# Optimization experiments

Measured on AMD Instinct MI355X. Metric: run time of the kernel, lower is better.

Reference implementation:

```python
import jax, jax.numpy as jnp
from jax import lax
import numpy as np

B, N, S, K = 8, 4096, 1024, 32
D_FEAT = 64
EPS = 1e-5


def fps_idx(pts, npoint):
    # pts: [N,3] -> farthest point sampling indices [npoint] (deterministic start at 0)
    n = pts.shape[0]
    def body(i, state):
        dist, far, idxs = state
        idxs = idxs.at[i].set(far)
        d = jnp.sum((pts - pts[far]) ** 2, axis=-1)
        dist = jnp.minimum(dist, d)
        return dist, jnp.argmax(dist).astype(jnp.int32), idxs
    init = (jnp.full((n,), 1e10, pts.dtype), jnp.int32(0), jnp.zeros((npoint,), jnp.int32))
    _, _, idxs = lax.fori_loop(0, npoint, body, init)
    return idxs


def bn(x, g, b, axes, c_axis):
    # batch-norm, training mode (batch statistics), matching torch default module state
    m = jnp.mean(x, axes, keepdims=True)
    v = jnp.var(x, axes, keepdims=True)
    shape = [1] * x.ndim
    shape[c_axis] = -1
    return g.reshape(shape) * (x - m) * lax.rsqrt(v + EPS) + b.reshape(shape)


def conv1x1(x, w, b):
    # x: [B,C,S,K], w: [O,C], b: [O]
    return jnp.einsum('oc,bcsk->bosk', w, x) + b[None, :, None, None]


def setup_inputs():
    key = jax.random.key(0)
    ks = jax.random.split(key, 20)
    p = lambda k, shape: jax.random.normal(k, shape, jnp.float32) * 0.05
    inp = {
        'xyz': jax.random.normal(ks[0], (B, 3, N), jnp.float32),
        'features': jax.random.normal(ks[1], (B, D_FEAT, N), jnp.float32),
        # main MLP: 67 -> 64 -> 64 -> 128
        'w0': p(ks[2], (64, 67)), 'b0': p(ks[3], (64,)), 'g0': jnp.ones(64), 'be0': jnp.zeros(64),
        'w1': p(ks[4], (64, 64)), 'b1': p(ks[5], (64,)), 'g1': jnp.ones(64), 'be1': jnp.zeros(64),
        'w2': p(ks[6], (128, 64)), 'b2': p(ks[7], (128,)), 'g2': jnp.ones(128), 'be2': jnp.zeros(128),
        # WeightNet: 3 -> 8 -> 8 -> 16
        'ww0': p(ks[8], (8, 3)), 'wb0': p(ks[9], (8,)), 'wg0': jnp.ones(8), 'wbe0': jnp.zeros(8),
        'ww1': p(ks[10], (8, 8)), 'wb1': p(ks[11], (8,)), 'wg1': jnp.ones(8), 'wbe1': jnp.zeros(8),
        'ww2': p(ks[12], (16, 8)), 'wb2': p(ks[13], (16,)), 'wg2': jnp.ones(16), 'wbe2': jnp.zeros(16),
        # final linear 16*128 -> 128 and BN1d
        'lw': p(ks[14], (128, 16 * 128)), 'lb': p(ks[15], (128,)),
        'lg': jnp.ones(128), 'lbe': jnp.zeros(128),
    }
    return inp


def reference(xyz, features, w0, b0, g0, be0, w1, b1, g1, be1, w2, b2, g2, be2,
              ww0, wb0, wg0, wbe0, ww1, wb1, wg1, wbe1, ww2, wb2, wg2, wbe2,
              lw, lb, lg, lbe):
    xyz_t = jnp.transpose(xyz, (0, 2, 1))          # [B,N,3]
    feat_t = jnp.transpose(features, (0, 2, 1))    # [B,N,D]

    # farthest point sampling (indices non-differentiable, as in CUDA FPS)
    fidx = jax.vmap(lambda pts: fps_idx(pts, S))(lax.stop_gradient(xyz_t))  # [B,S]
    fps_xyz = jnp.take_along_axis(xyz_t, fidx[..., None], axis=1)           # [B,S,3]

    # KNN: squared distances [B,S,N], take K smallest
    d2 = (jnp.sum(fps_xyz ** 2, -1, keepdims=True)
          + jnp.sum(xyz_t ** 2, -1)[:, None, :]
          - 2.0 * jnp.einsum('bsc,bnc->bsn', fps_xyz, xyz_t))
    _, idx = lax.top_k(-lax.stop_gradient(d2), K)                            # [B,S,K]

    gather = jax.vmap(lambda src, i: src[i])
    grouped_xyz = gather(xyz_t, idx) - fps_xyz[:, :, None, :]                # [B,S,K,3]
    grouped_feat = gather(feat_t, idx)                                       # [B,S,K,D]
    nf = jnp.concatenate([grouped_xyz, grouped_feat], axis=-1)               # [B,S,K,3+D]

    nf = jnp.transpose(nf, (0, 3, 1, 2))                                     # [B,C,S,K]
    for w, b, g, be in ((w0, b0, g0, be0), (w1, b1, g1, be1), (w2, b2, g2, be2)):
        nf = jax.nn.relu(bn(conv1x1(nf, w, b), g, be, (0, 2, 3), 1))

    gx = jnp.transpose(grouped_xyz, (0, 3, 1, 2))                            # [B,3,S,K]
    wts = gx
    for w, b, g, be in ((ww0, wb0, wg0, wbe0), (ww1, wb1, wg1, wbe1), (ww2, wb2, wg2, wbe2)):
        wts = jax.nn.relu(bn(conv1x1(wts, w, b), g, be, (0, 2, 3), 1))       # [B,16,S,K]

    agg = jnp.einsum('bdsk,bcsk->bsdc', nf, wts)                             # [B,S,128,16]
    agg = agg.reshape(agg.shape[0], agg.shape[1], -1)                        # [B,S,2048] (D outer, C inner)
    lin = agg @ lw.T + lb                                                    # [B,S,128]
    lin = jnp.transpose(lin, (0, 2, 1))                                      # [B,128,S]
    out_f = jax.nn.relu(bn(lin, lg, lbe, (0, 2), 1))

    new_xyz = jnp.transpose(fps_xyz, (0, 2, 1))                              # [B,3,S]
    return (new_xyz, out_f)
```

## Files before the change

kernel.cpp:

```cpp
#include <hip/hip_runtime.h>
#include <hip/hip_bf16.h>

#define BB 8
#define NN 4096
#define SS 1024
#define KK 32
#define PP (BB*SS*KK)

typedef unsigned long long u64;
typedef unsigned int u32;
typedef unsigned short u16;
typedef float f32x2 __attribute__((ext_vector_type(2)));

#define ST_Y0 0
#define ST_W0 64
#define ST_Y1 72
#define ST_W1 136
#define ST_Y2 144
#define ST_W2 272
#define ST_LIN 288

static __device__ __forceinline__ float bf2f(u32 u){ return __uint_as_float(u<<16); }
static __device__ __forceinline__ u16 f2bf(float f){ u32 u=__float_as_uint(f); return (u16)((u + 0x7FFFu + ((u>>16)&1u))>>16); }

static __device__ __forceinline__ f32x2 pk_add(f32x2 a, f32x2 b){
  f32x2 d; asm("v_pk_add_f32 %0, %1, %2" : "=v"(d) : "v"(a), "v"(b)); return d;
}
static __device__ __forceinline__ f32x2 pk_mul(f32x2 a, f32x2 b){
  f32x2 d; asm("v_pk_mul_f32 %0, %1, %2" : "=v"(d) : "v"(a), "v"(b)); return d;
}

static __device__ __forceinline__ uint4 pack8(const float* v){
  uint4 r;
  r.x=(u32)f2bf(v[0])|((u32)f2bf(v[1])<<16);
  r.y=(u32)f2bf(v[2])|((u32)f2bf(v[3])<<16);
  r.z=(u32)f2bf(v[4])|((u32)f2bf(v[5])<<16);
  r.w=(u32)f2bf(v[6])|((u32)f2bf(v[7])<<16);
  return r;
}

static __device__ __forceinline__ void unp8_aff(uint4 r, const float* A, const float* C, int cb, float* o){
  o[0]=fmaxf(fmaf(bf2f(r.x&0xffffu),A[cb+0],C[cb+0]),0.f);
  o[1]=fmaxf(fmaf(bf2f(r.x>>16)    ,A[cb+1],C[cb+1]),0.f);
  o[2]=fmaxf(fmaf(bf2f(r.y&0xffffu),A[cb+2],C[cb+2]),0.f);
  o[3]=fmaxf(fmaf(bf2f(r.y>>16)    ,A[cb+3],C[cb+3]),0.f);
  o[4]=fmaxf(fmaf(bf2f(r.z&0xffffu),A[cb+4],C[cb+4]),0.f);
  o[5]=fmaxf(fmaf(bf2f(r.z>>16)    ,A[cb+5],C[cb+5]),0.f);
  o[6]=fmaxf(fmaf(bf2f(r.w&0xffffu),A[cb+6],C[cb+6]),0.f);
  o[7]=fmaxf(fmaf(bf2f(r.w>>16)    ,A[cb+7],C[cb+7]),0.f);
}

template<int CTRL, int RMASK>
static __device__ __forceinline__ u32 dppmax(u32 m){
  u32 t=(u32)__builtin_amdgcn_update_dpp(0, (int)m, CTRL, RMASK, 0xf, false);
  return t>m ? t : m;
}
template<int CTRL, int RMASK>
static __device__ __forceinline__ float dppadd1(float v){
  float t=__uint_as_float((u32)__builtin_amdgcn_update_dpp(0,(int)__float_as_uint(v),CTRL,RMASK,0xf,false));
  return v+t;
}
static __device__ __forceinline__ float dppsum(float v){
  v=dppadd1<0x111,0xf>(v);
  v=dppadd1<0x112,0xf>(v);
  v=dppadd1<0x114,0xf>(v);
  v=dppadd1<0x118,0xf>(v);
  v=dppadd1<0x142,0xa>(v);
  v=dppadd1<0x143,0xc>(v);
  return v;
}
static __device__ __forceinline__ float rl63(float v){
  return __uint_as_float((u32)__builtin_amdgcn_readlane((int)__float_as_uint(v),63));
}

__global__ __launch_bounds__(512) void k_fps_ft(const float* __restrict__ xyz,
    float* __restrict__ fpsq, float* __restrict__ outx,
    const float* __restrict__ f, float* __restrict__ ft,
    const float* __restrict__ w0,const float* __restrict__ w1,const float* __restrict__ w2,
    const float* __restrict__ ww0,const float* __restrict__ ww1,const float* __restrict__ ww2,
    float* __restrict__ w0t,float* __restrict__ w1t,float* __restrict__ w2t,
    float* __restrict__ wt0,float* __restrict__ wt1,float* __restrict__ wt2,
    float* __restrict__ statsf){
  __shared__ union USm {
    struct { float X[NN],Y[NN],Z[NN]; float QX[SS],QY[SS],QZ[SS]; u64 red[2][8]; } a;
    float tile[2][64][65];
  } sm;
  int blk=blockIdx.x; int t=threadIdx.x;
  if (blk>=8){
    if (blk==264){
      for (int i=t;i<1024;i+=512) statsf[i]=0.f;
      for (int i=t;i<64*67;i+=512){ int o=i/67,k=i%67; w0t[k*64+o]=w0[i]; }
      for (int i=t;i<64*64;i+=512){ int o=i>>6,k=i&63; w1t[k*64+o]=w1[i]; }
      for (int i=t;i<128*64;i+=512){ int o=i>>6,k=i&63; w2t[k*128+o]=w2[i]; }
      for (int i=t;i<8*3;i+=512){ int o=i/3,k=i%3; wt0[k*8+o]=ww0[i]; }
      for (int i=t;i<8*8;i+=512){ int o=i>>3,k=i&7; wt1[k*8+o]=ww1[i]; }
      for (int i=t;i<16*8;i+=512){ int o=i>>3,k=i&7; wt2[k*16+o]=ww2[i]; }
      return;
    }
    int sub=t>>8, tt=t&255;
    int tileIdx=(blk-8)*2+sub;
    int b=tileIdx>>6; int n0=(tileIdx&63)*64;
    const float* fb=f+(size_t)b*64*NN;
    int c0=tt>>6, nn=tt&63;
    #pragma unroll
    for (int it=0;it<16;it++){ int c=c0+it*4; sm.tile[sub][c][nn]=fb[(size_t)c*NN+n0+nn]; }
    __syncthreads();
    int cc=tt&63, n1=tt>>6;
    float* fo=ft+((size_t)b*NN+n0)*64;
    #pragma unroll
    for (int it=0;it<16;it++){ int n=n1+it*4; fo[(size_t)n*64+cc]=sm.tile[sub][cc][n]; }
    return;
  }
  float* X=sm.a.X; float* Y=sm.a.Y; float* Z=sm.a.Z;
  float* QX=sm.a.QX; float* QY=sm.a.QY; float* QZ=sm.a.QZ;
  int b=blk;
  const float* xb=xyz+(size_t)b*3*NN;
  for (int i=t;i<NN;i+=512){ X[i]=xb[i]; Y[i]=xb[NN+i]; Z[i]=xb[2*NN+i]; }
  __syncthreads();
  f32x2 px[4],py[4],pz[4],dd[4];
  #pragma unroll
  for (int k=0;k<4;k++){
    int i=t*8+2*k;
    px[k].x=X[i]; px[k].y=X[i+1];
    py[k].x=Y[i]; py[k].y=Y[i+1];
    pz[k].x=Z[i]; pz[k].y=Z[i+1];
    dd[k].x=1e10f; dd[k].y=1e10f;
  }
  int wv=t>>6, ln=t&63;
  int far=0;
  for (int s=0;s<SS;s++){
    float fx=X[far], fy=Y[far], fz=Z[far];
    if (t==0){ QX[s]=fx; QY[s]=fy; QZ[s]=fz; }
    f32x2 nfx, nfy, nfz;
    nfx.x=-fx; nfx.y=-fx; nfy.x=-fy; nfy.y=-fy; nfz.x=-fz; nfz.y=-fz;
    #pragma unroll
    for (int k=0;k<4;k++){
      f32x2 dx=pk_add(px[k],nfx);
      f32x2 xx=pk_mul(dx,dx);
      f32x2 dy=pk_add(py[k],nfy);
      f32x2 yy=pk_mul(dy,dy);
      f32x2 dz=pk_add(pz[k],nfz);
      f32x2 zz=pk_mul(dz,dz);
      f32x2 s1=pk_add(xx,yy);
      f32x2 d2=pk_add(s1,zz);
      dd[k].x=fminf(dd[k].x,d2.x);
      dd[k].y=fminf(dd[k].y,d2.y);
    }
    float m01=fmaxf(dd[0].x,dd[0].y), m23=fmaxf(dd[1].x,dd[1].y);
    float m45=fmaxf(dd[2].x,dd[2].y), m67=fmaxf(dd[3].x,dd[3].y);
    u32 m=__float_as_uint(fmaxf(fmaxf(m01,m23),fmaxf(m45,m67)));
    m=dppmax<0x111,0xf>(m);
    m=dppmax<0x112,0xf>(m);
    m=dppmax<0x114,0xf>(m);
    m=dppmax<0x118,0xf>(m);
    u32 r15=(u32)__builtin_amdgcn_readlane((int)m,15);
    u32 r31=(u32)__builtin_amdgcn_readlane((int)m,31);
    u32 r47=(u32)__builtin_amdgcn_readlane((int)m,47);
    u32 r63=(u32)__builtin_amdgcn_readlane((int)m,63);
    u32 ab = r15>r31 ? r15 : r31;
    u32 cd = r47>r63 ? r47 : r63;
    u32 wmax = ab>cd ? ab : cd;
    int lj=8;
    if (__float_as_uint(dd[3].y)==wmax) lj=7;
    if (__float_as_uint(dd[3].x)==wmax) lj=6;
    if (__float_as_uint(dd[2].y)==wmax) lj=5;
    if (__float_as_uint(dd[2].x)==wmax) lj=4;
    if (__float_as_uint(dd[1].y)==wmax) lj=3;
    if (__float_as_uint(dd[1].x)==wmax) lj=2;
    if (__float_as_uint(dd[0].y)==wmax) lj=1;
    if (__float_as_uint(dd[0].x)==wmax) lj=0;
    u64 ball=__ballot(lj<8);
    u32 wl=(u32)__builtin_ctzll(ball);
    int gi=t*8+lj;
    u32 widx=(u32)__builtin_amdgcn_readlane(gi,wl);
    int pb=s&1;
    if (ln==0) sm.a.red[pb][wv]=((u64)wmax<<32)|(u32)(4095u-widx);
    __syncthreads();
    const double* rd=(const double*)&sm.a.red[pb][0];
    double g=fmax(fmax(fmax(rd[0],rd[1]),fmax(rd[2],rd[3])),
                  fmax(fmax(rd[4],rd[5]),fmax(rd[6],rd[7])));
    far=4095-(int)(__double_as_longlong(g)&0xFFFull);
  }
  __syncthreads();
  for (int i=t;i<SS;i+=512){
    float qx=QX[i], qy=QY[i], qz=QZ[i];
    float* q=&fpsq[((size_t)b*SS+i)*3]; q[0]=qx; q[1]=qy; q[2]=qz;
    outx[b*3*SS+i]=qx; outx[b*3*SS+SS+i]=qy; outx[b*3*SS+2*SS+i]=qz;
  }
}

#define KSTR 68
__global__ __launch_bounds__(256) void k_knn(const float* __restrict__ xyz, const float* __restrict__ fpsq,
                                             int* __restrict__ kidx){
  extern __shared__ char smem[];
  float* xs=(float*)smem;
  float* ys=xs+64*KSTR;
  float* zs=ys+64*KSTR;
  float* pn=zs+64*KSTR;
  int blk=blockIdx.x; int b=blk>>8; int s0=(blk&255)*4;
  const float* xb=xyz+(size_t)b*3*NN;
  for (int i=threadIdx.x;i<NN;i+=256){
    float x=xb[i],y=xb[NN+i],z=xb[2*NN+i];
    int slot=(i>>6)*KSTR+(i&63);
    xs[slot]=x; ys[slot]=y; zs[slot]=z;
    pn[slot]=__fadd_rn(__fadd_rn(__fmul_rn(x,x),__fmul_rn(y,y)),__fmul_rn(z,z));
  }
  __syncthreads();
  int wv=threadIdx.x>>6, ln=threadIdx.x&63;
  int s=s0+wv;
  const float* q=&fpsq[((size_t)b*SS+s)*3];
  float qx=q[0],qy=q[1],qz=q[2];
  float qn=__fadd_rn(__fadd_rn(__fmul_rn(qx,qx),__fmul_rn(qy,qy)),__fmul_rn(qz,qz));
  f32x2 qxx,qyy,qzz,qnn,mtwo;
  qxx.x=qx;qxx.y=qx; qyy.x=qy;qyy.y=qy; qzz.x=qz;qzz.y=qz; qnn.x=qn;qnn.y=qn;
  mtwo.x=-2.f; mtwo.y=-2.f;
  const float4* Xp=(const float4*)(xs+ln*KSTR);
  const float4* Yp=(const float4*)(ys+ln*KSTR);
  const float4* Zp=(const float4*)(zs+ln*KSTR);
  const float4* Pp=(const float4*)(pn+ln*KSTR);
  int base=ln*64;
  u64 v[64];
  #pragma unroll
  for (int g=0;g<16;g++){
    float4 x4=Xp[g], y4=Yp[g], z4=Zp[g], p4=Pp[g];
    #pragma unroll
    for (int h=0;h<2;h++){
      f32x2 px2,py2,pz2,pn2;
      if (h==0){ px2.x=x4.x;px2.y=x4.y; py2.x=y4.x;py2.y=y4.y; pz2.x=z4.x;pz2.y=z4.y; pn2.x=p4.x;pn2.y=p4.y; }
      else     { px2.x=x4.z;px2.y=x4.w; py2.x=y4.z;py2.y=y4.w; pz2.x=z4.z;pz2.y=z4.w; pn2.x=p4.z;pn2.y=p4.w; }
      f32x2 m1=pk_mul(qxx,px2);
      f32x2 mm=pk_mul(qyy,py2);
      f32x2 a1=pk_add(m1,mm);
      f32x2 m3=pk_mul(qzz,pz2);
      f32x2 dt=pk_add(a1,m3);
      f32x2 qp=pk_add(qnn,pn2);
      f32x2 nd=pk_mul(dt,mtwo);
      f32x2 d2=pk_add(qp,nd);
      #pragma unroll
      for (int e=0;e<2;e++){
        u32 bu=__float_as_uint(e?d2.y:d2.x);
        bu = ((int)bu<0)? ~bu : (bu|0x80000000u);
        v[g*4+h*2+e]=((u64)bu<<32)|(u32)(base+g*4+h*2+e);
      }
    }
  }
  u64 cand[8];
  #pragma unroll
  for (int gg=0;gg<8;gg++){
    u64 c=v[gg*8];
    #pragma unroll
    for (int j=1;j<8;j++){ u64 x=v[gg*8+j]; c = x<c?x:c; }
    cand[gg]=c;
  }
  u64 best=cand[0];
  #pragma unroll
  for (int gg=1;gg<8;gg++){ u64 x=cand[gg]; best = x<best?x:best; }
  int my=0;
  #pragma unroll 1
  for (int r=0;r<KK;r++){
    u64 w=best;
    #pragma unroll
    for (int m=1;m<64;m<<=1){ u64 o=__shfl_xor(w,m,64); w = o<w?o:w; }
    if (ln==r) my=(int)(w&0xFFFull);
    if (best==w){
      #pragma unroll
      for (int gg=0;gg<8;gg++){
        if (cand[gg]==w){
          u64 c=~0ull;
          #pragma unroll
          for (int j=0;j<8;j++){ u64 x=v[gg*8+j]; x = x>w ? x : ~0ull; c = x<c?x:c; }
          cand[gg]=c;
        }
      }
      u64 nb=cand[0];
      #pragma unroll
      for (int gg=1;gg<8;gg++){ u64 x=cand[gg]; nb = x<nb?x:nb; }
      best=nb;
    }
  }
  if (ln<KK) kidx[(((size_t)b*SS+s)<<5)+ln]=my;
}

__global__ __launch_bounds__(256) void k_l0(const float* __restrict__ xyz, const float* __restrict__ ft,
    const float* __restrict__ fpsq, const int* __restrict__ kidx,
    const float* __restrict__ w0t, const float* __restrict__ wt0,
    u16* __restrict__ y0, float* __restrict__ wl0, float* __restrict__ statsf){
  __shared__ u16 ytile[256][64];
  __shared__ float pS[4][64], pQ[4][64];
  __shared__ float pWS[4][8], pWQ[4][8];
  int t=threadIdx.x; int wv=t>>6, ln=t&63;
  int p=blockIdx.x*256+t;
  int b=p>>15;
  int site=p>>5;
  int j=kidx[p];
  const float* xb=xyz+(size_t)b*3*NN;
  const float* q=fpsq+(size_t)site*3;
  float gx=xb[j]-q[0], gy=xb[NN+j]-q[1], gz=xb[2*NN+j]-q[2];
  float acc[64];
  #pragma unroll
  for (int c=0;c<64;c++) acc[c]=fmaf(gx,w0t[c],fmaf(gy,w0t[64+c],gz*w0t[128+c]));
  const float4* fr=(const float4*)(ft+((size_t)b*NN+j)*64);
  #pragma unroll 1
  for (int kb=0;kb<4;kb++){
    float4 r0=fr[kb*4+0], r1=fr[kb*4+1], r2=fr[kb*4+2], r3=fr[kb*4+3];
    float ch[16]={r0.x,r0.y,r0.z,r0.w,r1.x,r1.y,r1.z,r1.w,r2.x,r2.y,r2.z,r2.w,r3.x,r3.y,r3.z,r3.w};
    const float* wb=w0t+(3+kb*16)*64;
    #pragma unroll
    for (int kk=0;kk<16;kk++){
      #pragma unroll
      for (int c=0;c<64;c++) acc[c]=fmaf(ch[kk],wb[kk*64+c],acc[c]);
    }
  }
  u16* yr=y0+(size_t)p*64;
  #pragma unroll
  for (int c8=0;c8<8;c8++){
    uint4 pk=pack8(&acc[c8*8]);
    ((uint4*)yr)[c8]=pk;
    *((uint4*)&ytile[t][c8*8])=pk;
  }
  float wa[8];
  #pragma unroll
  for (int o=0;o<8;o++) wa[o]=fmaf(gx,wt0[o],fmaf(gy,wt0[8+o],gz*wt0[16+o]));
  float4* wr=(float4*)(wl0+(size_t)p*8);
  wr[0]=make_float4(wa[0],wa[1],wa[2],wa[3]);
  wr[1]=make_float4(wa[4],wa[5],wa[6],wa[7]);
  float wS[8],wQ[8];
  #pragma unroll
  for (int o=0;o<8;o++){
    wS[o]=rl63(dppsum(wa[o]));
    wQ[o]=rl63(dppsum(wa[o]*wa[o]));
  }
  if (ln==0){
    #pragma unroll
    for (int o=0;o<8;o++){ pWS[wv][o]=wS[o]; pWQ[wv][o]=wQ[o]; }
  }
  __syncthreads();
  {
    int c=t&63, rg=t>>6;
    float S=0.f,Q=0.f;
    #pragma unroll 16
    for (int r=0;r<64;r++){
      float v=bf2f((u32)ytile[rg*64+r][c]);
      S+=v; Q=fmaf(v,v,Q);
    }
    pS[rg][c]=S; pQ[rg][c]=Q;
  }
  __syncthreads();
  if (t<64){
    float S=pS[0][t]+pS[1][t]+pS[2][t]+pS[3][t];
    float Q=pQ[0][t]+pQ[1][t]+pQ[2][t]+pQ[3][t];
    atomicAdd(&statsf[2*(ST_Y0+t)],S); atomicAdd(&statsf[2*(ST_Y0+t)+1],Q);
  } else if (t<72){
    int c=t-64;
    float S=pWS[0][c]+pWS[1][c]+pWS[2][c]+pWS[3][c];
    float Q=pWQ[0][c]+pWQ[1][c]+pWQ[2][c]+pWQ[3][c];
    atomicAdd(&statsf[2*(ST_W0+c)],S); atomicAdd(&statsf[2*(ST_W0+c)+1],Q);
  }
}

__global__ __launch_bounds__(256) void k_l1(const u16* __restrict__ y0, const float* __restrict__ wl0,
    const float* __restrict__ w1t, const float* __restrict__ wt1,
    const float* __restrict__ statsf,
    const float* __restrict__ g0v, const float* __restrict__ be0v,
    const float* __restrict__ wg0v, const float* __restrict__ wbe0v,
    u16* __restrict__ y1, float* __restrict__ wl1, float* __restrict__ statso){
  __shared__ float A0[64],C0[64],AW[8],CW[8];
  __shared__ u16 ytile[256][64];
  __shared__ float pS[4][64], pQ[4][64];
  __shared__ float pWS[4][8], pWQ[4][8];
  int t=threadIdx.x; int wv=t>>6, ln=t&63;
  if (t<64){
    float sm=statsf[(ST_Y0+t)*2], sq=statsf[(ST_Y0+t)*2+1];
    float mean=sm*(1.f/PP), var=fmaxf(sq*(1.f/PP)-mean*mean,0.f);
    float a=g0v[t]*rsqrtf(var+1e-5f); A0[t]=a; C0[t]=be0v[t]-mean*a;
  } else if (t<72){
    int c=t-64;
    float sm=statsf[(ST_W0+c)*2], sq=statsf[(ST_W0+c)*2+1];
    float mean=sm*(1.f/PP), var=fmaxf(sq*(1.f/PP)-mean*mean,0.f);
    float a=wg0v[c]*rsqrtf(var+1e-5f); AW[c]=a; CW[c]=wbe0v[c]-mean*a;
  }
  __syncthreads();
  int p=blockIdx.x*256+t;
  const uint4* yr=(const uint4*)(y0+(size_t)p*64);
  float acc[64];
  #pragma unroll
  for (int c=0;c<64;c++) acc[c]=0.f;
  #pragma unroll 1
  for (int kb=0;kb<4;kb++){
    uint4 r0=yr[kb*2], r1=yr[kb*2+1];
    float ch[16];
    unp8_aff(r0,A0,C0,kb*16,ch);
    unp8_aff(r1,A0,C0,kb*16+8,ch+8);
    const float* wb=w1t+kb*16*64;
    #pragma unroll
    for (int kk=0;kk<16;kk++){
      #pragma unroll
      for (int c=0;c<64;c++) acc[c]=fmaf(ch[kk],wb[kk*64+c],acc[c]);
    }
  }
  u16* yo=y1+(size_t)p*64;
  #pragma unroll
  for (int c8=0;c8<8;c8++){
    uint4 pk=pack8(&acc[c8*8]);
    ((uint4*)yo)[c8]=pk;
    *((uint4*)&ytile[t][c8*8])=pk;
  }
  const float4* wvp=(const float4*)(wl0+(size_t)p*8);
  float4 v0=wvp[0], v1=wvp[1];
  float wi[8]={v0.x,v0.y,v0.z,v0.w,v1.x,v1.y,v1.z,v1.w};
  float wo[8];
  #pragma unroll
  for (int o=0;o<8;o++) wo[o]=0.f;
  #pragma unroll
  for (int k=0;k<8;k++){
    float xr=fmaxf(fmaf(wi[k],AW[k],CW[k]),0.f);
    #pragma unroll
    for (int o=0;o<8;o++) wo[o]=fmaf(xr,wt1[k*8+o],wo[o]);
  }
  float4* wr=(float4*)(wl1+(size_t)p*8);
  wr[0]=make_float4(wo[0],wo[1],wo[2],wo[3]);
  wr[1]=make_float4(wo[4],wo[5],wo[6],wo[7]);
  float wS[8],wQ[8];
  #pragma unroll
  for (int o=0;o<8;o++){
    wS[o]=rl63(dppsum(wo[o]));
    wQ[o]=rl63(dppsum(wo[o]*wo[o]));
  }
  if (ln==0){
    #pragma unroll
    for (int o=0;o<8;o++){ pWS[wv][o]=wS[o]; pWQ[wv][o]=wQ[o]; }
  }
  __syncthreads();
  {
    int c=t&63, rg=t>>6;
    float S=0.f,Q=0.f;
    #pragma unroll 16
    for (int r=0;r<64;r++){
      float v=bf2f((u32)ytile[rg*64+r][c]);
      S+=v; Q=fmaf(v,v,Q);
    }
    pS[rg][c]=S; pQ[rg][c]=Q;
  }
  __syncthreads();
  if (t<64){
    float S=pS[0][t]+pS[1][t]+pS[2][t]+pS[3][t];
    float Q=pQ[0][t]+pQ[1][t]+pQ[2][t]+pQ[3][t];
    atomicAdd(&statso[2*(ST_Y1+t)],S); atomicAdd(&statso[2*(ST_Y1+t)+1],Q);
  } else if (t<72){
    int c=t-64;
    float S=pWS[0][c]+pWS[1][c]+pWS[2][c]+pWS[3][c];
    float Q=pWQ[0][c]+pWQ[1][c]+pWQ[2][c]+pWQ[3][c];
    atomicAdd(&statso[2*(ST_W1+c)],S); atomicAdd(&statso[2*(ST_W1+c)+1],Q);
  }
}

__global__ __launch_bounds__(256) void k_l2(const u16* __restrict__ y1, const float* __restrict__ wl1,
    const float* __restrict__ w2t, const float* __restrict__ wt2,
    const float* __restrict__ statsf,
    const float* __restrict__ g1v, const float* __restrict__ be1v,
    const float* __restrict__ wg1v, const float* __restrict__ wbe1v,
    u16* __restrict__ y2, float* __restrict__ wl2, float* __restrict__ statso){
  __shared__ float A1[64],C1[64],AW[8],CW[8];
  __shared__ u16 ytile[256][64];
  __shared__ float pS[4][64], pQ[4][64];
  __shared__ float pWS[4][16], pWQ[4][16];
  int t=threadIdx.x; int wv=t>>6, ln=t&63;
  if (t<64){
    float sm=statsf[(ST_Y1+t)*2], sq=statsf[(ST_Y1+t)*2+1];
    float mean=sm*(1.f/PP), var=fmaxf(sq*(1.f/PP)-mean*mean,0.f);
    float a=g1v[t]*rsqrtf(var+1e-5f); A1[t]=a; C1[t]=be1v[t]-mean*a;
  } else if (t<72){
    int c=t-64;
    float sm=statsf[(ST_W1+c)*2], sq=statsf[(ST_W1+c)*2+1];
    float mean=sm*(1.f/PP), var=fmaxf(sq*(1.f/PP)-mean*mean,0.f);
    float a=wg1v[c]*rsqrtf(var+1e-5f); AW[c]=a; CW[c]=wbe1v[c]-mean*a;
  }
  __syncthreads();
  int p=blockIdx.x*256+t;
  const uint4* yr=(const uint4*)(y1+(size_t)p*64);
  #pragma unroll 1
  for (int h=0;h<2;h++){
    float acc[64];
    #pragma unroll
    for (int c=0;c<64;c++) acc[c]=0.f;
    #pragma unroll 1
    for (int kb=0;kb<4;kb++){
      uint4 r0=yr[kb*2], r1=yr[kb*2+1];
      float ch[16];
      unp8_aff(r0,A1,C1,kb*16,ch);
      unp8_aff(r1,A1,C1,kb*16+8,ch+8);
      const float* wb=w2t+(size_t)kb*16*128+h*64;
      #pragma unroll
      for (int kk=0;kk<16;kk++){
        #pragma unroll
        for (int c=0;c<64;c++) acc[c]=fmaf(ch[kk],wb[kk*128+c],acc[c]);
      }
    }
    u16* yo=y2+(size_t)p*128+h*64;
    #pragma unroll
    for (int c8=0;c8<8;c8++){
      uint4 pk=pack8(&acc[c8*8]);
      ((uint4*)yo)[c8]=pk;
      *((uint4*)&ytile[t][c8*8])=pk;
    }
    __syncthreads();
    {
      int c=t&63, rg=t>>6;
      float S=0.f,Q=0.f;
      #pragma unroll 16
      for (int r=0;r<64;r++){
        float v=bf2f((u32)ytile[rg*64+r][c]);
        S+=v; Q=fmaf(v,v,Q);
      }
      pS[rg][c]=S; pQ[rg][c]=Q;
    }
    __syncthreads();
    if (t<64){
      float S=pS[0][t]+pS[1][t]+pS[2][t]+pS[3][t];
      float Q=pQ[0][t]+pQ[1][t]+pQ[2][t]+pQ[3][t];
      atomicAdd(&statso[2*(ST_Y2+h*64+t)],S); atomicAdd(&statso[2*(ST_Y2+h*64+t)+1],Q);
    }
    __syncthreads();
  }
  const float4* wvp=(const float4*)(wl1+(size_t)p*8);
  float4 v0=wvp[0], v1=wvp[1];
  float wi[8]={v0.x,v0.y,v0.z,v0.w,v1.x,v1.y,v1.z,v1.w};
  float wo[16];
  #pragma unroll
  for (int o=0;o<16;o++) wo[o]=0.f;
  #pragma unroll
  for (int k=0;k<8;k++){
    float xr=fmaxf(fmaf(wi[k],AW[k],CW[k]),0.f);
    #pragma unroll
    for (int o=0;o<16;o++) wo[o]=fmaf(xr,wt2[k*16+o],wo[o]);
  }
  float4* wr=(float4*)(wl2+(size_t)p*16);
  wr[0]=make_float4(wo[0],wo[1],wo[2],wo[3]);
  wr[1]=make_float4(wo[4],wo[5],wo[6],wo[7]);
  wr[2]=make_float4(wo[8],wo[9],wo[10],wo[11]);
  wr[3]=make_float4(wo[12],wo[13],wo[14],wo[15]);
  float wS[16],wQ[16];
  #pragma unroll
  for (int o=0;o<16;o++){
    wS[o]=rl63(dppsum(wo[o]));
    wQ[o]=rl63(dppsum(wo[o]*wo[o]));
  }
  if (ln==0){
    #pragma unroll
    for (int o=0;o<16;o++){ pWS[wv][o]=wS[o]; pWQ[wv][o]=wQ[o]; }
  }
  __syncthreads();
  if (t<16){
    float S=pWS[0][t]+pWS[1][t]+pWS[2][t]+pWS[3][t];
    float Q=pWQ[0][t]+pWQ[1][t]+pWQ[2][t]+pWQ[3][t];
    atomicAdd(&statso[2*(ST_W2+t)],S); atomicAdd(&statso[2*(ST_W2+t)+1],Q);
  }
}

__global__ __launch_bounds__(256) void k_agg(const u16* __restrict__ y2, const float* __restrict__ wl2,
    const float* __restrict__ statsf,
    const float* __restrict__ g2v, const float* __restrict__ be2v,
    const float* __restrict__ wg2v, const float* __restrict__ wbe2v,
    u16* __restrict__ agg){
  __shared__ float A2[128],C2[128],AW[16],CW[16];
  __shared__ float nf[32*128];
  __shared__ float wt[32*16];
  int site=blockIdx.x; int t=threadIdx.x;
  if (t<128){
    float sm=statsf[(ST_Y2+t)*2], sq=statsf[(ST_Y2+t)*2+1];
    float mean=sm*(1.f/PP), var=fmaxf(sq*(1.f/PP)-mean*mean,0.f);
    float a=g2v[t]*rsqrtf(var+1e-5f); A2[t]=a; C2[t]=be2v[t]-mean*a;
  } else if (t<144){
    int c=t-128;
    float sm=statsf[(ST_W2+c)*2], sq=statsf[(ST_W2+c)*2+1];
    float mean=sm*(1.f/PP), var=fmaxf(sq*(1.f/PP)-mean*mean,0.f);
    float a=wg2v[c]*rsqrtf(var+1e-5f); AW[c]=a; CW[c]=wbe2v[c]-mean*a;
  }
  __syncthreads();
  const uint4* src=(const uint4*)(y2+(size_t)site*32*128);
  #pragma unroll
  for (int it=0;it<2;it++){
    int idx=t+it*256;
    uint4 r=src[idx];
    int base=(idx*8)&127; int kq=(idx*8)>>7;
    unp8_aff(r,A2,C2,base,&nf[kq*128+base]);
  }
  #pragma unroll
  for (int it=0;it<2;it++){
    int i=t+it*256;
    float x=wl2[(size_t)site*512+i]; int c=i&15;
    wt[i]=fmaxf(fmaf(x,AW[c],CW[c]),0.f);
  }
  __syncthreads();
  int d=t>>1, cb=(t&1)*8;
  float acc[8];
  #pragma unroll
  for (int e=0;e<8;e++) acc[e]=0.f;
  #pragma unroll 4
  for (int kq=0;kq<32;kq++){
    float nv=nf[kq*128+d];
    #pragma unroll
    for (int e=0;e<8;e++) acc[e]=fmaf(nv,wt[kq*16+cb+e],acc[e]);
  }
  ((uint4*)(agg+(size_t)site*2048))[t]=pack8(acc);
}

__global__ __launch_bounds__(256) void k_lin(const u16* __restrict__ agg, const float* __restrict__ lw,
                                             float* __restrict__ lin, float* __restrict__ outst){
  __shared__ float As[32][33];
  __shared__ float Bs[32][128];
  __shared__ float stS[8][132], stQ[8][132];
  int s0=blockIdx.x*32; int t=threadIdx.x;
  int tx=t&31, ty=t>>5;
  float acc[4][4];
  #pragma unroll
  for (int i=0;i<4;i++){
    #pragma unroll
    for (int jj=0;jj<4;jj++) acc[i][jj]=0.f;
  }
  for (int kb=0;kb<2048;kb+=32){
    {
      int row=t>>3, kc=(t&7)*4;
      uint2 raw=*(const uint2*)(agg+((size_t)(s0+row))*2048+kb+kc);
      As[row][kc  ]=bf2f(raw.x&0xffffu); As[row][kc+1]=bf2f(raw.x>>16);
      As[row][kc+2]=bf2f(raw.y&0xffffu); As[row][kc+3]=bf2f(raw.y>>16);
    }
    {
      int o=t>>1, ks=(t&1)*16;
      const float* lr=lw+(size_t)o*2048+kb+ks;
      #pragma unroll
      for (int i=0;i<16;i+=4){
        float4 r=*(const float4*)(lr+i);
        Bs[ks+i][o]=r.x; Bs[ks+i+1][o]=r.y; Bs[ks+i+2][o]=r.z; Bs[ks+i+3][o]=r.w;
      }
    }
    __syncthreads();
    #pragma unroll 8
    for (int kk=0;kk<32;kk++){
      float av[4];
      #pragma unroll
      for (int i=0;i<4;i++) av[i]=As[ty*4+i][kk];
      float4 bv=*(const float4*)(&Bs[kk][tx*4]);
      #pragma unroll
      for (int i=0;i<4;i++){
        acc[i][0]=fmaf(av[i],bv.x,acc[i][0]);
        acc[i][1]=fmaf(av[i],bv.y,acc[i][1]);
        acc[i][2]=fmaf(av[i],bv.z,acc[i][2]);
        acc[i][3]=fmaf(av[i],bv.w,acc[i][3]);
      }
    }
    __syncthreads();
  }
  #pragma unroll
  for (int i=0;i<4;i++){
    float4 o4=make_float4(acc[i][0],acc[i][1],acc[i][2],acc[i][3]);
    *(float4*)(lin+((size_t)(s0+ty*4+i))*128+tx*4)=o4;
  }
  #pragma unroll
  for (int jj=0;jj<4;jj++){
    float a0=acc[0][jj],a1=acc[1][jj],a2=acc[2][jj],a3=acc[3][jj];
    stS[ty][tx*4+jj]=(a0+a1)+(a2+a3);
    stQ[ty][tx*4+jj]=fmaf(a3,a3,fmaf(a2,a2,fmaf(a1,a1,a0*a0)));
  }
  __syncthreads();
  if (t<128){
    float S=0.f,Q=0.f;
    #pragma unroll
    for (int k=0;k<8;k++){ S+=stS[k][t]; Q+=stQ[k][t]; }
    atomicAdd(&outst[2*t],S); atomicAdd(&outst[2*t+1],Q);
  }
}

__global__ __launch_bounds__(256) void k_out(const float* __restrict__ lin, const float* __restrict__ statsf,
    const float* __restrict__ lg, const float* __restrict__ lbe, float* __restrict__ outf){
  int t=blockIdx.x*256+threadIdx.x;
  int s4=(t&255)*4; int o=(t>>8)&127; int b=t>>15;
  float sm=statsf[(ST_LIN+o)*2], sq=statsf[(ST_LIN+o)*2+1];
  float mean=sm*(1.f/8192.f), var=fmaxf(sq*(1.f/8192.f)-mean*mean,0.f);
  float a=lg[o]*rsqrtf(var+1e-5f), cc=lbe[o]-mean*a;
  float v0=lin[((size_t)b*SS+s4+0)*128+o];
  float v1=lin[((size_t)b*SS+s4+1)*128+o];
  float v2=lin[((size_t)b*SS+s4+2)*128+o];
  float v3=lin[((size_t)b*SS+s4+3)*128+o];
  float4 r=make_float4(fmaxf(fmaf(v0,a,cc),0.f),fmaxf(fmaf(v1,a,cc),0.f),
                       fmaxf(fmaf(v2,a,cc),0.f),fmaxf(fmaf(v3,a,cc),0.f));
  *(float4*)(outf+((size_t)b*128+o)*SS+s4)=r;
}

extern "C" void kernel_launch(void* const* d_in, const int* in_sizes, int n_in,
                              void* d_out, int out_size, void* d_ws, size_t ws_size,
                              hipStream_t stream){
  (void)in_sizes;(void)n_in;(void)out_size;(void)ws_size;
  const float* xyz =(const float*)d_in[0];
  const float* feat=(const float*)d_in[1];
  const float* w0=(const float*)d_in[2];  const float* g0=(const float*)d_in[4];  const float* be0=(const float*)d_in[5];
  const float* w1=(const float*)d_in[6];  const float* g1=(const float*)d_in[8];  const float* be1=(const float*)d_in[9];
  const float* w2=(const float*)d_in[10]; const float* g2=(const float*)d_in[12]; const float* be2=(const float*)d_in[13];
  const float* ww0=(const float*)d_in[14]; const float* wg0=(const float*)d_in[16]; const float* wbe0=(const float*)d_in[17];
  const float* ww1=(const float*)d_in[18]; const float* wg1=(const float*)d_in[20]; const float* wbe1=(const float*)d_in[21];
  const float* ww2=(const float*)d_in[22]; const float* wg2=(const float*)d_in[24]; const float* wbe2=(const float*)d_in[25];
  const float* lw=(const float*)d_in[26]; const float* lg=(const float*)d_in[28]; const float* lbe=(const float*)d_in[29];
  float* out=(float*)d_out;
  char* ws=(char*)d_ws;

  size_t cur=0;
  auto alloc=[&](size_t bytes)->size_t{ cur=(cur+255)&~(size_t)255; size_t o=cur; cur+=bytes; return o; };
  size_t o_stats=alloc(4096);
  size_t o_w0t =alloc(67*64*4);
  size_t o_w1t =alloc(64*64*4);
  size_t o_w2t =alloc(64*128*4);
  size_t o_wt0 =alloc(3*8*4);
  size_t o_wt1 =alloc(8*8*4);
  size_t o_wt2 =alloc(8*16*4);
  size_t o_fpsq=alloc((size_t)BB*SS*3*4);
  size_t o_kidx=alloc((size_t)PP*4);
  size_t o_ft  =alloc((size_t)BB*NN*64*4);
  size_t o_y0  =alloc((size_t)PP*64*2);
  size_t o_y1  =alloc((size_t)PP*64*2);
  size_t o_y2  =alloc((size_t)PP*128*2);
  size_t o_wl0 =alloc((size_t)PP*8*4);
  size_t o_wl1 =alloc((size_t)PP*8*4);
  size_t o_wl2 =alloc((size_t)PP*16*4);
  size_t o_agg =alloc((size_t)8192*2048*2);
  size_t o_lin =alloc((size_t)8192*128*4);

  float* statsf=(float*)(ws+o_stats);
  float* w0t=(float*)(ws+o_w0t); float* w1t=(float*)(ws+o_w1t); float* w2t=(float*)(ws+o_w2t);
  float* wt0=(float*)(ws+o_wt0); float* wt1=(float*)(ws+o_wt1); float* wt2=(float*)(ws+o_wt2);
  float* fpsq=(float*)(ws+o_fpsq); int* kidx=(int*)(ws+o_kidx);
  float* ft=(float*)(ws+o_ft);
  u16* y0=(u16*)(ws+o_y0); u16* y1=(u16*)(ws+o_y1); u16* y2=(u16*)(ws+o_y2);
  float* wl0=(float*)(ws+o_wl0); float* wl1=(float*)(ws+o_wl1); float* wl2=(float*)(ws+o_wl2);
  u16* agg=(u16*)(ws+o_agg); float* lin=(float*)(ws+o_lin);

  size_t knn_smem = (size_t)4*64*KSTR*4;

  hipLaunchKernelGGL(k_fps_ft,dim3(265),dim3(512),0,stream,xyz,fpsq,out,feat,ft,
                     w0,w1,w2,ww0,ww1,ww2,w0t,w1t,w2t,wt0,wt1,wt2,statsf);
  hipLaunchKernelGGL(k_knn,dim3(2048),dim3(256),knn_smem,stream,xyz,fpsq,kidx);
  hipLaunchKernelGGL(k_l0,dim3(PP/256),dim3(256),0,stream,xyz,ft,fpsq,kidx,w0t,wt0,y0,wl0,statsf);
  hipLaunchKernelGGL(k_l1,dim3(PP/256),dim3(256),0,stream,y0,wl0,w1t,wt1,statsf,g0,be0,wg0,wbe0,y1,wl1,statsf);
  hipLaunchKernelGGL(k_l2,dim3(PP/256),dim3(256),0,stream,y1,wl1,w2t,wt2,statsf,g1,be1,wg1,wbe1,y2,wl2,statsf);
  hipLaunchKernelGGL(k_agg,dim3(8192),dim3(256),0,stream,y2,wl2,statsf,g2,be2,wg2,wbe2,agg);
  hipLaunchKernelGGL(k_lin,dim3(256),dim3(256),0,stream,agg,lw,lin,statsf+2*ST_LIN);
  hipLaunchKernelGGL(k_out,dim3(1024),dim3(256),0,stream,lin,statsf,lg,lbe,out+BB*3*SS);
}
```

Measured before the change: 1.315 ms.

## Fuse all stages into one cooperative persistent kernel with grid syncs

Replaces the eight separate kernel launches with a single cooperative kernel of 256 blocks of 512 threads that runs FPS, kNN, the three MLP layers, aggregation, the linear layer and the output BN in sequence, separated by grid.sync. The aim is to remove launch gaps and per-kernel tail effects. Work is remapped onto the fixed grid, with two passes per stage and kNN handling 32 queries per block. The cost is that 248 blocks sit idle during the long serial FPS phase, and the smaller grid may lower occupancy and parallelism in the heavier stages.

After: 2.262 ms. 71.9% more time.

```diff
diff --git a/kernel.cpp b/kernel.cpp
--- a/kernel.cpp
+++ b/kernel.cpp
@@ -1,5 +1,8 @@
 #include <hip/hip_runtime.h>
 #include <hip/hip_bf16.h>
+#include <hip/hip_cooperative_groups.h>
+
+namespace cg = cooperative_groups;
 
 #define BB 8
 #define NN 4096
@@ -20,8 +23,13 @@
 #define ST_W2 272
 #define ST_LIN 288
 
+#define DLDS 69632
+#define KSTR 68
+
 static __device__ __forceinline__ float bf2f(u32 u){ return __uint_as_float(u<<16); }
 static __device__ __forceinline__ u16 f2bf(float f){ u32 u=__float_as_uint(f); return (u16)((u + 0x7FFFu + ((u>>16)&1u))>>16); }
+
+static __device__ __forceinline__ float aread(float* p){ return atomicAdd(p, 0.0f); }
 
 static __device__ __forceinline__ f32x2 pk_add(f32x2 a, f32x2 b){
   f32x2 d; asm("v_pk_add_f32 %0, %1, %2" : "=v"(d) : "v"(a), "v"(b)); return d;
@@ -73,21 +81,129 @@
   return __uint_as_float((u32)__builtin_amdgcn_readlane((int)__float_as_uint(v),63));
 }
 
-__global__ __launch_bounds__(512) void k_fps_ft(const float* __restrict__ xyz,
-    float* __restrict__ fpsq, float* __restrict__ outx,
-    const float* __restrict__ f, float* __restrict__ ft,
+__global__ __launch_bounds__(512,2) void k_mega(
+    const float* __restrict__ xyz, const float* __restrict__ feat,
     const float* __restrict__ w0,const float* __restrict__ w1,const float* __restrict__ w2,
     const float* __restrict__ ww0,const float* __restrict__ ww1,const float* __restrict__ ww2,
-    float* __restrict__ w0t,float* __restrict__ w1t,float* __restrict__ w2t,
-    float* __restrict__ wt0,float* __restrict__ wt1,float* __restrict__ wt2,
-    float* __restrict__ statsf){
-  __shared__ union USm {
-    struct { float X[NN],Y[NN],Z[NN]; float QX[SS],QY[SS],QZ[SS]; u64 red[2][8]; } a;
-    float tile[2][64][65];
-  } sm;
-  int blk=blockIdx.x; int t=threadIdx.x;
-  if (blk>=8){
-    if (blk==264){
+    const float* __restrict__ g0,const float* __restrict__ be0,
+    const float* __restrict__ g1,const float* __restrict__ be1,
+    const float* __restrict__ g2,const float* __restrict__ be2,
+    const float* __restrict__ wg0,const float* __restrict__ wbe0,
+    const float* __restrict__ wg1,const float* __restrict__ wbe1,
+    const float* __restrict__ wg2,const float* __restrict__ wbe2,
+    const float* __restrict__ lw,const float* __restrict__ lg,const float* __restrict__ lbe,
+    float* out,
+    float* fpsq, int* kidx, float* ft,
+    u16* y0, u16* y1, u16* y2,
+    float* wl0, float* wl1, float* wl2,
+    u16* aggb, float* lin, float* statsf,
+    float* w0t, float* w1t, float* w2t,
+    float* wt0, float* wt1, float* wt2){
+  extern __shared__ char dsm[];
+  __shared__ union SSM {
+    u64 red[2][8];
+    struct { float pS[8][64], pQ[8][64], pWS[8][16], pWQ[8][16];
+             float A[64], C[64], AW[8], CW[8]; } st;
+    struct { float A[128], C[128], AW[16], CW[16]; } bn;
+    struct { float S[128], Q2[128]; } ln;
+  } ssm;
+  cg::grid_group grid = cg::this_grid();
+  const int blk=blockIdx.x, t=threadIdx.x;
+  const int wv=t>>6, ln=t&63;
+
+  if (blk<8){
+    float* X=(float*)dsm; float* Y=X+NN; float* Z=Y+NN;
+    float* QX=Z+NN; float* QY=QX+SS; float* QZ=QY+SS;
+    const float* xb=xyz+(size_t)blk*3*NN;
+    for (int i=t;i<NN;i+=512){ X[i]=xb[i]; Y[i]=xb[NN+i]; Z[i]=xb[2*NN+i]; }
+    __syncthreads();
+    f32x2 px[4],py[4],pz[4],dd[4];
+    #pragma unroll
+    for (int k=0;k<4;k++){
+      int i=t*8+2*k;
+      px[k].x=X[i]; px[k].y=X[i+1];
+      py[k].x=Y[i]; py[k].y=Y[i+1];
+      pz[k].x=Z[i]; pz[k].y=Z[i+1];
+      dd[k].x=1e10f; dd[k].y=1e10f;
+    }
+    int far=0;
+    for (int s=0;s<SS;s++){
+      float fx=X[far], fy=Y[far], fz=Z[far];
+      if (t==0){ QX[s]=fx; QY[s]=fy; QZ[s]=fz; }
+      f32x2 nfx, nfy, nfz;
+      nfx.x=-fx; nfx.y=-fx; nfy.x=-fy; nfy.y=-fy; nfz.x=-fz; nfz.y=-fz;
+      #pragma unroll
+      for (int k=0;k<4;k++){
+        f32x2 dx=pk_add(px[k],nfx);
+        f32x2 xx=pk_mul(dx,dx);
+        f32x2 dy=pk_add(py[k],nfy);
+        f32x2 yy=pk_mul(dy,dy);
+        f32x2 dz=pk_add(pz[k],nfz);
+        f32x2 zz=pk_mul(dz,dz);
+        f32x2 s1=pk_add(xx,yy);
+        f32x2 d2=pk_add(s1,zz);
+        dd[k].x=fminf(dd[k].x,d2.x);
+        dd[k].y=fminf(dd[k].y,d2.y);
+      }
+      float m01=fmaxf(dd[0].x,dd[0].y), m23=fmaxf(dd[1].x,dd[1].y);
+      float m45=fmaxf(dd[2].x,dd[2].y), m67=fmaxf(dd[3].x,dd[3].y);
+      u32 m=__float_as_uint(fmaxf(fmaxf(m01,m23),fmaxf(m45,m67)));
+      m=dppmax<0x111,0xf>(m);
+      m=dppmax<0x112,0xf>(m);
+      m=dppmax<0x114,0xf>(m);
+      m=dppmax<0x118,0xf>(m);
+      u32 r15=(u32)__builtin_amdgcn_readlane((int)m,15);
+      u32 r31=(u32)__builtin_amdgcn_readlane((int)m,31);
+      u32 r47=(u32)__builtin_amdgcn_readlane((int)m,47);
+      u32 r63=(u32)__builtin_amdgcn_readlane((int)m,63);
+      u32 ab = r15>r31 ? r15 : r31;
+      u32 cd = r47>r63 ? r47 : r63;
+      u32 wmax = ab>cd ? ab : cd;
+      int lj=8;
+      if (__float_as_uint(dd[3].y)==wmax) lj=7;
+      if (__float_as_uint(dd[3].x)==wmax) lj=6;
+      if (__float_as_uint(dd[2].y)==wmax) lj=5;
+      if (__float_as_uint(dd[2].x)==wmax) lj=4;
+      if (__float_as_uint(dd[1].y)==wmax) lj=3;
+      if (__float_as_uint(dd[1].x)==wmax) lj=2;
+      if (__float_as_uint(dd[0].y)==wmax) lj=1;
+      if (__float_as_uint(dd[0].x)==wmax) lj=0;
+      u64 ball=__ballot(lj<8);
+      u32 wl=(u32)__builtin_ctzll(ball);
+      int gi=t*8+lj;
+      u32 widx=(u32)__builtin_amdgcn_readlane(gi,wl);
+      int pb=s&1;
+      if (ln==0) ssm.red[pb][wv]=((u64)wmax<<32)|(u32)(4095u-widx);
+      __syncthreads();
+      const double* rd=(const double*)&ssm.red[pb][0];
+      double g=fmax(fmax(fmax(rd[0],rd[1]),fmax(rd[2],rd[3])),
+                    fmax(fmax(rd[4],rd[5]),fmax(rd[6],rd[7])));
+      far=4095-(int)(__double_as_longlong(g)&0xFFFull);
+    }
+    __syncthreads();
+    for (int i=t;i<SS;i+=512){
+      float qx=QX[i], qy=QY[i], qz=QZ[i];
+      float* q=&fpsq[((size_t)blk*SS+i)*3]; q[0]=qx; q[1]=qy; q[2]=qz;
+      out[blk*3*SS+i]=qx; out[blk*3*SS+SS+i]=qy; out[blk*3*SS+2*SS+i]=qz;
+    }
+  } else {
+    float (*tile)[64][65]=(float(*)[64][65])dsm;
+    int sub=t>>8, tt=t&255;
+    for (int base=blk-8; base<256; base+=248){
+      int tileIdx=base*2+sub;
+      int b=tileIdx>>6; int n0=(tileIdx&63)*64;
+      const float* fb=feat+(size_t)b*64*NN;
+      int c0=tt>>6, nn=tt&63;
+      #pragma unroll
+      for (int it=0;it<16;it++){ int c=c0+it*4; tile[sub][c][nn]=fb[(size_t)c*NN+n0+nn]; }
+      __syncthreads();
+      int cc=tt&63, n1=tt>>6;
+      float* fo=ft+((size_t)b*NN+n0)*64;
+      #pragma unroll
+      for (int it=0;it<16;it++){ int n=n1+it*4; fo[(size_t)n*64+cc]=tile[sub][cc][n]; }
+      __syncthreads();
+    }
+    if (blk==254){
       for (int i=t;i<1024;i+=512) statsf[i]=0.f;
       for (int i=t;i<64*67;i+=512){ int o=i/67,k=i%67; w0t[k*64+o]=w0[i]; }
       for (int i=t;i<64*64;i+=512){ int o=i>>6,k=i&63; w1t[k*64+o]=w1[i]; }
@@ -95,596 +211,497 @@
       for (int i=t;i<8*3;i+=512){ int o=i/3,k=i%3; wt0[k*8+o]=ww0[i]; }
       for (int i=t;i<8*8;i+=512){ int o=i>>3,k=i&7; wt1[k*8+o]=ww1[i]; }
       for (int i=t;i<16*8;i+=512){ int o=i>>3,k=i&7; wt2[k*16+o]=ww2[i]; }
-      return;
-    }
+    }
+  }
+  __threadfence(); grid.sync();
+
+  {
+    float* xs=(float*)dsm;
+    float* ys=xs+64*KSTR;
+    float* zs=ys+64*KSTR;
+    float* pn=zs+64*KSTR;
+    int b=blk>>5; int q0=(blk&31)<<5;
+    const float* xb=xyz+(size_t)b*3*NN;
+    for (int i=t;i<NN;i+=512){
+      float x=xb[i],y=xb[NN+i],z=xb[2*NN+i];
+      int slot=(i>>6)*KSTR+(i&63);
+      xs[slot]=x; ys[slot]=y; zs[slot]=z;
+      pn[slot]=__fadd_rn(__fadd_rn(__fmul_rn(x,x),__fmul_rn(y,y)),__fmul_rn(z,z));
+    }
+    __syncthreads();
+    const float4* Xp=(const float4*)(xs+ln*KSTR);
+    const float4* Yp=(const float4*)(ys+ln*KSTR);
+    const float4* Zp=(const float4*)(zs+ln*KSTR);
+    const float4* Pp=(const float4*)(pn+ln*KSTR);
+    int base=ln*64;
+    #pragma unroll 1
+    for (int pass=0;pass<4;pass++){
+      int s=q0+pass*8+wv;
+      const float* q=&fpsq[((size_t)b*SS+s)*3];
+      float qx=q[0],qy=q[1],qz=q[2];
+      float qn=__fadd_rn(__fadd_rn(__fmul_rn(qx,qx),__fmul_rn(qy,qy)),__fmul_rn(qz,qz));
+      f32x2 qxx,qyy,qzz,qnn,mtwo;
+      qxx.x=qx;qxx.y=qx; qyy.x=qy;qyy.y=qy; qzz.x=qz;qzz.y=qz; qnn.x=qn;qnn.y=qn;
+      mtwo.x=-2.f; mtwo.y=-2.f;
+      u64 v[64];
+      #pragma unroll
+      for (int g=0;g<16;g++){
+        float4 x4=Xp[g], y4=Yp[g], z4=Zp[g], p4=Pp[g];
+        #pragma unroll
+        for (int h=0;h<2;h++){
+          f32x2 px2,py2,pz2,pn2;
+          if (h==0){ px2.x=x4.x;px2.y=x4.y; py2.x=y4.x;py2.y=y4.y; pz2.x=z4.x;pz2.y=z4.y; pn2.x=p4.x;pn2.y=p4.y; }
+          else     { px2.x=x4.z;px2.y=x4.w; py2.x=y4.z;py2.y=y4.w; pz2.x=z4.z;pz2.y=z4.w; pn2.x=p4.z;pn2.y=p4.w; }
+          f32x2 m1=pk_mul(qxx,px2);
+          f32x2 mm=pk_mul(qyy,py2);
+          f32x2 a1=pk_add(m1,mm);
+          f32x2 m3=pk_mul(qzz,pz2);
+          f32x2 dt=pk_add(a1,m3);
+          f32x2 qp=pk_add(qnn,pn2);
+          f32x2 nd=pk_mul(dt,mtwo);
+          f32x2 d2=pk_add(qp,nd);
+          #pragma unroll
+          for (int e=0;e<2;e++){
+            u32 bu=__float_as_uint(e?d2.y:d2.x);
+            bu = ((int)bu<0)? ~bu : (bu|0x80000000u);
+            v[g*4+h*2+e]=((u64)bu<<32)|(u32)(base+g*4+h*2+e);
+          }
+        }
+      }
+      u64 cand[8];
+      #pragma unroll
+      for (int gg=0;gg<8;gg++){
+        u64 c=v[gg*8];
+        #pragma unroll
+        for (int j=1;j<8;j++){ u64 x=v[gg*8+j]; c = x<c?x:c; }
+        cand[gg]=c;
+      }
+      u64 best=cand[0];
+      #pragma unroll
+      for (int gg=1;gg<8;gg++){ u64 x=cand[gg]; best = x<best?x:best; }
+      int my=0;
+      #pragma unroll 1
+      for (int r=0;r<KK;r++){
+        u64 w=best;
+        #pragma unroll
+        for (int m=1;m<64;m<<=1){ u64 o=__shfl_xor(w,m,64); w = o<w?o:w; }
+        if (ln==r) my=(int)(w&0xFFFull);
+        if (best==w){
+          #pragma unroll
+          for (int gg=0;gg<8;gg++){
+            if (cand[gg]==w){
+              u64 c=~0ull;
+              #pragma unroll
+              for (int j=0;j<8;j++){ u64 x=v[gg*8+j]; x = x>w ? x : ~0ull; c = x<c?x:c; }
+              cand[gg]=c;
+            }
+          }
+          u64 nb=cand[0];
+          #pragma unroll
+          for (int gg=1;gg<8;gg++){ u64 x=cand[gg]; nb = x<nb?x:nb; }
+          best=nb;
+        }
+      }
+      if (ln<KK) kidx[(((size_t)b*SS+s)<<5)+ln]=my;
+    }
+  }
+  __threadfence(); grid.sync();
+
+  {
+    u16 (*ytile)[64]=(u16(*)[64])dsm;
+    #pragma unroll 1
+    for (int pass=0;pass<2;pass++){
+      int p=blk*512+t+pass*131072;
+      int b=p>>15;
+      int site=p>>5;
+      int j=kidx[p];
+      const float* xb=xyz+(size_t)b*3*NN;
+      const float* q=fpsq+(size_t)site*3;
+      float gx=xb[j]-q[0], gy=xb[NN+j]-q[1], gz=xb[2*NN+j]-q[2];
+      float acc[64];
+      #pragma unroll
+      for (int c=0;c<64;c++) acc[c]=fmaf(gx,w0t[c],fmaf(gy,w0t[64+c],gz*w0t[128+c]));
+      const float4* fr=(const float4*)(ft+((size_t)b*NN+j)*64);
+      #pragma unroll 1
+      for (int kb=0;kb<4;kb++){
+        float4 r0=fr[kb*4+0], r1=fr[kb*4+1], r2=fr[kb*4+2], r3=fr[kb*4+3];
+        float ch[16]={r0.x,r0.y,r0.z,r0.w,r1.x,r1.y,r1.z,r1.w,r2.x,r2.y,r2.z,r2.w,r3.x,r3.y,r3.z,r3.w};
+        const float* wb=w0t+(3+kb*16)*64;
+        #pragma unroll
+        for (int kk=0;kk<16;kk++){
+          #pragma unroll
+          for (int c=0;c<64;c++) acc[c]=fmaf(ch[kk],wb[kk*64+c],acc[c]);
+        }
+      }
+      u16* yr=y0+(size_t)p*64;
+      #pragma unroll
+      for (int c8=0;c8<8;c8++){
+        uint4 pk=pack8(&acc[c8*8]);
+        ((uint4*)yr)[c8]=pk;
+        *((uint4*)&ytile[t][c8*8])=pk;
+      }
+      float wa[8];
+      #pragma unroll
+      for (int o=0;o<8;o++) wa[o]=fmaf(gx,wt0[o],fmaf(gy,wt0[8+o],gz*wt0[16+o]));
+      float4* wr=(float4*)(wl0+(size_t)p*8);
+      wr[0]=make_float4(wa[0],wa[1],wa[2],wa[3]);
+      wr[1]=make_float4(wa[4],wa[5],wa[6],wa[7]);
+      float wS[8],wQ[8];
+      #pragma unroll
+      for (int o=0;o<8;o++){
+        wS[o]=rl63(dppsum(wa[o]));
+        wQ[o]=rl63(dppsum(wa[o]*wa[o]));
+      }
+      if (ln==0){
+        #pragma unroll
+        for (int o=0;o<8;o++){ ssm.st.pWS[wv][o]=wS[o]; ssm.st.pWQ[wv][o]=wQ[o]; }
+      }
+      __syncthreads();
+      {
+        int c=t&63, rg=t>>6;
+        float S=0.f,Q=0.f;
+        #pragma unroll 16
+        for (int r=0;r<64;r++){
+          float v=bf2f((u32)ytile[rg*64+r][c]);
+          S+=v; Q=fmaf(v,v,Q);
+        }
+        ssm.st.pS[rg][c]=S; ssm.st.pQ[rg][c]=Q;
+      }
+      __syncthreads();
+      if (t<64){
+        float S=0.f,Q=0.f;
+        #pragma unroll
+        for (int w=0;w<8;w++){ S+=ssm.st.pS[w][t]; Q+=ssm.st.pQ[w][t]; }
+        atomicAdd(&statsf[2*(ST_Y0+t)],S); atomicAdd(&statsf[2*(ST_Y0+t)+1],Q);
+      } else if (t<72){
+        int c=t-64;
+        float S=0.f,Q=0.f;
+        #pragma unroll
+        for (int w=0;w<8;w++){ S+=ssm.st.pWS[w][c]; Q+=ssm.st.pWQ[w][c]; }
+        atomicAdd(&statsf[2*(ST_W0+c)],S); atomicAdd(&statsf[2*(ST_W0+c)+1],Q);
+      }
+      __syncthreads();
+    }
+  }
+  __threadfence(); grid.sync();
+
+  {
+    u16 (*ytile)[64]=(u16(*)[64])dsm;
+    if (t<64){
+      float sm=aread(&statsf[(ST_Y0+t)*2]), sq=aread(&statsf[(ST_Y0+t)*2+1]);
+      float mean=sm*(1.f/PP), var=fmaxf(sq*(1.f/PP)-mean*mean,0.f);
+      float a=g0[t]*rsqrtf(var+1e-5f); ssm.st.A[t]=a; ssm.st.C[t]=be0[t]-mean*a;
+    } else if (t<72){
+      int c=t-64;
+      float sm=aread(&statsf[(ST_W0+c)*2]), sq=aread(&statsf[(ST_W0+c)*2+1]);
+      float mean=sm*(1.f/PP), var=fmaxf(sq*(1.f/PP)-mean*mean,0.f);
+      float a=wg0[c]*rsqrtf(var+1e-5f); ssm.st.AW[c]=a; ssm.st.CW[c]=wbe0[c]-mean*a;
+    }
+    __syncthreads();
+    #pragma unroll 1
+    for (int pass=0;pass<2;pass++){
+      int p=blk*512+t+pass*131072;
+      const uint4* yr=(const uint4*)(y0+(size_t)p*64);
+      float acc[64];
+      #pragma unroll
+      for (int c=0;c<64;c++) acc[c]=0.f;
+      #pragma unroll 1
+      for (int kb=0;kb<4;kb++){
+        uint4 r0=yr[kb*2], r1=yr[kb*2+1];
+        float ch[16];
+        unp8_aff(r0,ssm.st.A,ssm.st.C,kb*16,ch);
+        unp8_aff(r1,ssm.st.A,ssm.st.C,kb*16+8,ch+8);
+        const float* wb=w1t+kb*16*64;
+        #pragma unroll
+        for (int kk=0;kk<16;kk++){
+          #pragma unroll
+          for (int c=0;c<64;c++) acc[c]=fmaf(ch[kk],wb[kk*64+c],acc[c]);
+        }
+      }
+      u16* yo=y1+(size_t)p*64;
+      #pragma unroll
+      for (int c8=0;c8<8;c8++){
+        uint4 pk=pack8(&acc[c8*8]);
+        ((uint4*)yo)[c8]=pk;
+        *((uint4*)&ytile[t][c8*8])=pk;
+      }
+      const float4* wvp=(const float4*)(wl0+(size_t)p*8);
+      float4 v0=wvp[0], v1=wvp[1];
+      float wi[8]={v0.x,v0.y,v0.z,v0.w,v1.x,v1.y,v1.z,v1.w};
+      float wo[8];
+      #pragma unroll
+      for (int o=0;o<8;o++) wo[o]=0.f;
+      #pragma unroll
+      for (int k=0;k<8;k++){
+        float xr=fmaxf(fmaf(wi[k],ssm.st.AW[k],ssm.st.CW[k]),0.f);
+        #pragma unroll
+        for (int o=0;o<8;o++) wo[o]=fmaf(xr,wt1[k*8+o],wo[o]);
+      }
+      float4* wr=(float4*)(wl1+(size_t)p*8);
+      wr[0]=make_float4(wo[0],wo[1],wo[2],wo[3]);
+      wr[1]=make_float4(wo[4],wo[5],wo[6],wo[7]);
+      float wS[8],wQ[8];
+      #pragma unroll
+      for (int o=0;o<8;o++){
+        wS[o]=rl63(dppsum(wo[o]));
+        wQ[o]=rl63(dppsum(wo[o]*wo[o]));
+      }
+      if (ln==0){
+        #pragma unroll
+        for (int o=0;o<8;o++){ ssm.st.pWS[wv][o]=wS[o]; ssm.st.pWQ[wv][o]=wQ[o]; }
+      }
+      __syncthreads();
+      {
+        int c=t&63, rg=t>>6;
+        float S=0.f,Q=0.f;
+        #pragma unroll 16
+        for (int r=0;r<64;r++){
+          float v=bf2f((u32)ytile[rg*64+r][c]);
+          S+=v; Q=fmaf(v,v,Q);
+        }
+        ssm.st.pS[rg][c]=S; ssm.st.pQ[rg][c]=Q;
+      }
+      __syncthreads();
+      if (t<64){
+        float S=0.f,Q=0.f;
+        #pragma unroll
+        for (int w=0;w<8;w++){ S+=ssm.st.pS[w][t]; Q+=ssm.st.pQ[w][t]; }
+        atomicAdd(&statsf[2*(ST_Y1+t)],S); atomicAdd(&statsf[2*(ST_Y1+t)+1],Q);
+      } else if (t<72){
+        int c=t-64;
+        float S=0.f,Q=0.f;
+        #pragma unroll
+        for (int w=0;w<8;w++){ S+=ssm.st.pWS[w][c]; Q+=ssm.st.pWQ[w][c]; }
+        atomicAdd(&statsf[2*(ST_W1+c)],S); atomicAdd(&statsf[2*(ST_W1+c)+1],Q);
+      }
+      __syncthreads();
+    }
+  }
+  __threadfence(); grid.sync();
+
+  {
+    u16 (*ytile)[64]=(u16(*)[64])dsm;
+    if (t<64){
+      float sm=aread(&statsf[(ST_Y1+t)*2]), sq=aread(&statsf[(ST_Y1+t)*2+1]);
+      float mean=sm*(1.f/PP), var=fmaxf(sq*(1.f/PP)-mean*mean,0.f);
+      float a=g1[t]*rsqrtf(var+1e-5f); ssm.st.A[t]=a; ssm.st.C[t]=be1[t]-mean*a;
+    } else if (t<72){
+      int c=t-64;
+      float sm=aread(&statsf[(ST_W1+c)*2]), sq=aread(&statsf[(ST_W1+c)*2+1]);
+      float mean=sm*(1.f/PP), var=fmaxf(sq*(1.f/PP)-mean*mean,0.f);
+      float a=wg1[c]*rsqrtf(var+1e-5f); ssm.st.AW[c]=a; ssm.st.CW[c]=wbe1[c]-mean*a;
+    }
+    __syncthreads();
+    #pragma unroll 1
+    for (int pass=0;pass<2;pass++){
+      int p=blk*512+t+pass*131072;
+      const uint4* yr=(const uint4*)(y1+(size_t)p*64);
+      #pragma unroll 1
+      for (int h=0;h<2;h++){
+        float acc[64];
+        #pragma unroll
+        for (int c=0;c<64;c++) acc[c]=0.f;
+        #pragma unroll 1
+        for (int kb=0;kb<4;kb++){
+          uint4 r0=yr[kb*2], r1=yr[kb*2+1];
+          float ch[16];
+          unp8_aff(r0,ssm.st.A,ssm.st.C,kb*16,ch);
+          unp8_aff(r1,ssm.st.A,ssm.st.C,kb*16+8,ch+8);
+          const float* wb=w2t+(size_t)kb*16*128+h*64;
+          #pragma unroll
+          for (int kk=0;kk<16;kk++){
+            #pragma unroll
+            for (int c=0;c<64;c++) acc[c]=fmaf(ch[kk],wb[kk*128+c],acc[c]);
+          }
+        }
+        u16* yo=y2+(size_t)p*128+h*64;
+        #pragma unroll
+        for (int c8=0;c8<8;c8++){
+          uint4 pk=pack8(&acc[c8*8]);
+          ((uint4*)yo)[c8]=pk;
+          *((uint4*)&ytile[t][c8*8])=pk;
+        }
+        __syncthreads();
+        {
+          int c=t&63, rg=t>>6;
+          float S=0.f,Q=0.f;
+          #pragma unroll 16
+          for (int r=0;r<64;r++){
+            float v=bf2f((u32)ytile[rg*64+r][c]);
+            S+=v; Q=fmaf(v,v,Q);
+          }
+          ssm.st.pS[rg][c]=S; ssm.st.pQ[rg][c]=Q;
+        }
+        __syncthreads();
+        if (t<64){
+          float S=0.f,Q=0.f;
+          #pragma unroll
+          for (int w=0;w<8;w++){ S+=ssm.st.pS[w][t]; Q+=ssm.st.pQ[w][t]; }
+          atomicAdd(&statsf[2*(ST_Y2+h*64+t)],S); atomicAdd(&statsf[2*(ST_Y2+h*64+t)+1],Q);
+        }
+        __syncthreads();
+      }
+      const float4* wvp=(const float4*)(wl1+(size_t)p*8);
+      float4 v0=wvp[0], v1=wvp[1];
+      float wi[8]={v0.x,v0.y,v0.z,v0.w,v1.x,v1.y,v1.z,v1.w};
+      float wo[16];
+      #pragma unroll
+      for (int o=0;o<16;o++) wo[o]=0.f;
+      #pragma unroll
+      for (int k=0;k<8;k++){
+        float xr=fmaxf(fmaf(wi[k],ssm.st.AW[k],ssm.st.CW[k]),0.f);
+        #pragma unroll
+        for (int o=0;o<16;o++) wo[o]=fmaf(xr,wt2[k*16+o],wo[o]);
+      }
+      float4* wr=(float4*)(wl2+(size_t)p*16);
+      wr[0]=make_float4(wo[0],wo[1],wo[2],wo[3]);
+      wr[1]=make_float4(wo[4],wo[5],wo[6],wo[7]);
+      wr[2]=make_float4(wo[8],wo[9],wo[10],wo[11]);
+      wr[3]=make_float4(wo[12],wo[13],wo[14],wo[15]);
+      float wS[16],wQ[16];
+      #pragma unroll
+      for (int o=0;o<16;o++){
+        wS[o]=rl63(dppsum(wo[o]));
+        wQ[o]=rl63(dppsum(wo[o]*wo[o]));
+      }
+      if (ln==0){
+        #pragma unroll
+        for (int o=0;o<16;o++){ ssm.st.pWS[wv][o]=wS[o]; ssm.st.pWQ[wv][o]=wQ[o]; }
+      }
+      __syncthreads();
+      if (t<16){
+        float S=0.f,Q=0.f;
+        #pragma unroll
+        for (int w=0;w<8;w++){ S+=ssm.st.pWS[w][t]; Q+=ssm.st.pWQ[w][t]; }
+        atomicAdd(&statsf[2*(ST_W2+t)],S); atomicAdd(&statsf[2*(ST_W2+t)+1],Q);
+      }
+      __syncthreads();
+    }
+  }
+  __threadfence(); grid.sync();
+
+  {
+    if (t<128){
+      float sm=aread(&statsf[(ST_Y2+t)*2]), sq=aread(&statsf[(ST_Y2+t)*2+1]);
+      float mean=sm*(1.f/PP), var=fmaxf(sq*(1.f/PP)-mean*mean,0.f);
+      float a=g2[t]*rsqrtf(var+1e-5f); ssm.bn.A[t]=a; ssm.bn.C[t]=be2[t]-mean*a;
+    } else if (t<144){
+      int c=t-128;
+      float sm=aread(&statsf[(ST_W2+c)*2]), sq=aread(&statsf[(ST_W2+c)*2+1]);
+      float mean=sm*(1.f/PP), var=fmaxf(sq*(1.f/PP)-mean*mean,0.f);
+      float a=wg2[c]*rsqrtf(var+1e-5f); ssm.bn.AW[c]=a; ssm.bn.CW[c]=wbe2[c]-mean*a;
+    }
+    __syncthreads();
     int sub=t>>8, tt=t&255;
-    int tileIdx=(blk-8)*2+sub;
-    int b=tileIdx>>6; int n0=(tileIdx&63)*64;
-    const float* fb=f+(size_t)b*64*NN;
-    int c0=tt>>6, nn=tt&63;
-    #pragma unroll
-    for (int it=0;it<16;it++){ int c=c0+it*4; sm.tile[sub][c][nn]=fb[(size_t)c*NN+n0+nn]; }
+    float* nf=(float*)dsm + sub*4096;
+    float* wtb=(float*)dsm + 8192 + sub*512;
+    #pragma unroll 1
+    for (int it2=0;it2<16;it2++){
+      int site=blk*32+it2*2+sub;
+      const uint4* src=(const uint4*)(y2+(size_t)site*4096);
+      #pragma unroll
+      for (int it=0;it<2;it++){
+        int idx=tt+it*256;
+        uint4 r=src[idx];
+        int cb2=(idx*8)&127; int kq=(idx*8)>>7;
+        unp8_aff(r,ssm.bn.A,ssm.bn.C,cb2,&nf[kq*128+cb2]);
+      }
+      #pragma unroll
+      for (int it=0;it<2;it++){
+        int i=tt+it*256;
+        float x=wl2[(size_t)site*512+i]; int c=i&15;
+        wtb[i]=fmaxf(fmaf(x,ssm.bn.AW[c],ssm.bn.CW[c]),0.f);
+      }
+      __syncthreads();
+      int d=tt>>1, cb=(tt&1)*8;
+      float acc[8];
+      #pragma unroll
+      for (int e=0;e<8;e++) acc[e]=0.f;
+      #pragma unroll 4
+      for (int kq=0;kq<32;kq++){
+        float nv=nf[kq*128+d];
+        #pragma unroll
+        for (int e=0;e<8;e++) acc[e]=fmaf(nv,wtb[kq*16+cb+e],acc[e]);
+      }
+      ((uint4*)(aggb+(size_t)site*2048))[tt]=pack8(acc);
+      __syncthreads();
+    }
+  }
+  __threadfence(); grid.sync();
+
+  {
+    float (*As)[33]=(float(*)[33])dsm;
+    float (*Bs)[128]=(float(*)[128])(dsm+4224);
+    float (*stS)[132]=(float(*)[132])(dsm+20608);
+    float (*stQ)[132]=(float(*)[132])(dsm+29056);
+    int s0=blk*32; int tx=t&31, ty=t>>5;
+    float a00=0.f,a01=0.f,a02=0.f,a03=0.f;
+    float a10=0.f,a11=0.f,a12=0.f,a13=0.f;
+    #pragma unroll 1
+    for (int kb=0;kb<2048;kb+=32){
+      {
+        int row=t>>4, kc=(t&15)<<1;
+        u32 raw=*(const u32*)(aggb+((size_t)(s0+row))*2048+kb+kc);
+        As[row][kc]=bf2f(raw&0xffffu); As[row][kc+1]=bf2f(raw>>16);
+      }
+      {
+        int o=t>>2, ks=(t&3)*8;
+        const float* lr=lw+(size_t)o*2048+kb+ks;
+        float4 r1=*(const float4*)lr, r2=*(const float4*)(lr+4);
+        Bs[ks+0][o]=r1.x; Bs[ks+1][o]=r1.y; Bs[ks+2][o]=r1.z; Bs[ks+3][o]=r1.w;
+        Bs[ks+4][o]=r2.x; Bs[ks+5][o]=r2.y; Bs[ks+6][o]=r2.z; Bs[ks+7][o]=r2.w;
+      }
+      __syncthreads();
+      #pragma unroll 8
+      for (int kk=0;kk<32;kk++){
+        float av0=As[ty*2][kk], av1=As[ty*2+1][kk];
+        float4 bv=*(const float4*)(&Bs[kk][tx*4]);
+        a00=fmaf(av0,bv.x,a00); a01=fmaf(av0,bv.y,a01);
+        a02=fmaf(av0,bv.z,a02); a03=fmaf(av0,bv.w,a03);
+        a10=fmaf(av1,bv.x,a10); a11=fmaf(av1,bv.y,a11);
+        a12=fmaf(av1,bv.z,a12); a13=fmaf(av1,bv.w,a13);
+      }
+      __syncthreads();
+    }
+    *(float4*)(lin+((size_t)(s0+ty*2  ))*128+tx*4)=make_float4(a00,a01,a02,a03);
+    *(float4*)(lin+((size_t)(s0+ty*2+1))*128+tx*4)=make_float4(a10,a11,a12,a13);
+    stS[ty][tx*4+0]=a00+a10; stQ[ty][tx*4+0]=fmaf(a10,a10,a00*a00);
+    stS[ty][tx*4+1]=a01+a11; stQ[ty][tx*4+1]=fmaf(a11,a11,a01*a01);
+    stS[ty][tx*4+2]=a02+a12; stQ[ty][tx*4+2]=fmaf(a12,a12,a02*a02);
+    stS[ty][tx*4+3]=a03+a13; stQ[ty][tx*4+3]=fmaf(a13,a13,a03*a03);
     __syncthreads();
-    int cc=tt&63, n1=tt>>6;
-    float* fo=ft+((size_t)b*NN+n0)*64;
-    #pragma unroll
-    for (int it=0;it<16;it++){ int n=n1+it*4; fo[(size_t)n*64+cc]=sm.tile[sub][cc][n]; }
-    return;
+    if (t<128){
+      float S=0.f,Q=0.f;
+      #pragma unroll
+      for (int k=0;k<16;k++){ S+=stS[k][t]; Q+=stQ[k][t]; }
+      atomicAdd(&statsf[2*(ST_LIN+t)],S); atomicAdd(&statsf[2*(ST_LIN+t)+1],Q);
+    }
   }
-  float* X=sm.a.X; float* Y=sm.a.Y; float* Z=sm.a.Z;
-  float* QX=sm.a.QX; float* QY=sm.a.QY; float* QZ=sm.a.QZ;
-  int b=blk;
-  const float* xb=xyz+(size_t)b*3*NN;
-  for (int i=t;i<NN;i+=512){ X[i]=xb[i]; Y[i]=xb[NN+i]; Z[i]=xb[2*NN+i]; }
-  __syncthreads();
-  f32x2 px[4],py[4],pz[4],dd[4];
-  #pragma unroll
-  for (int k=0;k<4;k++){
-    int i=t*8+2*k;
-    px[k].x=X[i]; px[k].y=X[i+1];
-    py[k].x=Y[i]; py[k].y=Y[i+1];
-    pz[k].x=Z[i]; pz[k].y=Z[i+1];
-    dd[k].x=1e10f; dd[k].y=1e10f;
+  __threadfence(); grid.sync();
+
+  {
+    if (t<128){
+      ssm.ln.S[t] =aread(&statsf[(ST_LIN+t)*2]);
+      ssm.ln.Q2[t]=aread(&statsf[(ST_LIN+t)*2+1]);
+    }
+    __syncthreads();
+    float* outf=out+BB*3*SS;
+    #pragma unroll 1
+    for (int pass=0;pass<2;pass++){
+      int gt=blk*512+t+pass*131072;
+      int s4=(gt&255)*4; int o=(gt>>8)&127; int b=gt>>15;
+      float sm=ssm.ln.S[o], sq=ssm.ln.Q2[o];
+      float mean=sm*(1.f/8192.f), var=fmaxf(sq*(1.f/8192.f)-mean*mean,0.f);
+      float a=lg[o]*rsqrtf(var+1e-5f), cc=lbe[o]-mean*a;
+      float v0=lin[((size_t)b*SS+s4+0)*128+o];
+      float v1=lin[((size_t)b*SS+s4+1)*128+o];
+      float v2=lin[((size_t)b*SS+s4+2)*128+o];
+      float v3=lin[((size_t)b*SS+s4+3)*128+o];
+      float4 r=make_float4(fmaxf(fmaf(v0,a,cc),0.f),fmaxf(fmaf(v1,a,cc),0.f),
+                           fmaxf(fmaf(v2,a,cc),0.f),fmaxf(fmaf(v3,a,cc),0.f));
+      *(float4*)(outf+((size_t)b*128+o)*SS+s4)=r;
+    }
   }
-  int wv=t>>6, ln=t&63;
-  int far=0;
-  for (int s=0;s<SS;s++){
-    float fx=X[far], fy=Y[far], fz=Z[far];
-    if (t==0){ QX[s]=fx; QY[s]=fy; QZ[s]=fz; }
-    f32x2 nfx, nfy, nfz;
-    nfx.x=-fx; nfx.y=-fx; nfy.x=-fy; nfy.y=-fy; nfz.x=-fz; nfz.y=-fz;
-    #pragma unroll
-    for (int k=0;k<4;k++){
-      f32x2 dx=pk_add(px[k],nfx);
-      f32x2 xx=pk_mul(dx,dx);
-      f32x2 dy=pk_add(py[k],nfy);
-      f32x2 yy=pk_mul(dy,dy);
-      f32x2 dz=pk_add(pz[k],nfz);
-      f32x2 zz=pk_mul(dz,dz);
-      f32x2 s1=pk_add(xx,yy);
-      f32x2 d2=pk_add(s1,zz);
-      dd[k].x=fminf(dd[k].x,d2.x);
-      dd[k].y=fminf(dd[k].y,d2.y);
-    }
-    float m01=fmaxf(dd[0].x,dd[0].y), m23=fmaxf(dd[1].x,dd[1].y);
-    float m45=fmaxf(dd[2].x,dd[2].y), m67=fmaxf(dd[3].x,dd[3].y);
-    u32 m=__float_as_uint(fmaxf(fmaxf(m01,m23),fmaxf(m45,m67)));
-    m=dppmax<0x111,0xf>(m);
-    m=dppmax<0x112,0xf>(m);
-    m=dppmax<0x114,0xf>(m);
-    m=dppmax<0x118,0xf>(m);
-    u32 r15=(u32)__builtin_amdgcn_readlane((int)m,15);
-    u32 r31=(u32)__builtin_amdgcn_readlane((int)m,31);
-    u32 r47=(u32)__builtin_amdgcn_readlane((int)m,47);
-    u32 r63=(u32)__builtin_amdgcn_readlane((int)m,63);
-    u32 ab = r15>r31 ? r15 : r31;
-    u32 cd = r47>r63 ? r47 : r63;
-    u32 wmax = ab>cd ? ab : cd;
-    int lj=8;
-    if (__float_as_uint(dd[3].y)==wmax) lj=7;
-    if (__float_as_uint(dd[3].x)==wmax) lj=6;
-    if (__float_as_uint(dd[2].y)==wmax) lj=5;
-    if (__float_as_uint(dd[2].x)==wmax) lj=4;
-    if (__float_as_uint(dd[1].y)==wmax) lj=3;
-    if (__float_as_uint(dd[1].x)==wmax) lj=2;
-    if (__float_as_uint(dd[0].y)==wmax) lj=1;
-    if (__float_as_uint(dd[0].x)==wmax) lj=0;
-    u64 ball=__ballot(lj<8);
-    u32 wl=(u32)__builtin_ctzll(ball);
-    int gi=t*8+lj;
-    u32 widx=(u32)__builtin_amdgcn_readlane(gi,wl);
-    int pb=s&1;
-    if (ln==0) sm.a.red[pb][wv]=((u64)wmax<<32)|(u32)(4095u-widx);
-    __syncthreads();
-    const double* rd=(const double*)&sm.a.red[pb][0];
-    double g=fmax(fmax(fmax(rd[0],rd[1]),fmax(rd[2],rd[3])),
-                  fmax(fmax(rd[4],rd[5]),fmax(rd[6],rd[7])));
-    far=4095-(int)(__double_as_longlong(g)&0xFFFull);
-  }
-  __syncthreads();
-  for (int i=t;i<SS;i+=512){
-    float qx=QX[i], qy=QY[i], qz=QZ[i];
-    float* q=&fpsq[((size_t)b*SS+i)*3]; q[0]=qx; q[1]=qy; q[2]=qz;
-    outx[b*3*SS+i]=qx; outx[b*3*SS+SS+i]=qy; outx[b*3*SS+2*SS+i]=qz;
-  }
-}
-
-#define KSTR 68
-__global__ __launch_bounds__(256) void k_knn(const float* __restrict__ xyz, const float* __restrict__ fpsq,
-                                             int* __restrict__ kidx){
-  extern __shared__ char smem[];
-  float* xs=(float*)smem;
-  float* ys=xs+64*KSTR;
-  float* zs=ys+64*KSTR;
-  float* pn=zs+64*KSTR;
-  int blk=blockIdx.x; int b=blk>>8; int s0=(blk&255)*4;
-  const float* xb=xyz+(size_t)b*3*NN;
-  for (int i=threadIdx.x;i<NN;i+=256){
-    float x=xb[i],y=xb[NN+i],z=xb[2*NN+i];
-    int slot=(i>>6)*KSTR+(i&63);
-    xs[slot]=x; ys[slot]=y; zs[slot]=z;
-    pn[slot]=__fadd_rn(__fadd_rn(__fmul_rn(x,x),__fmul_rn(y,y)),__fmul_rn(z,z));
-  }
-  __syncthreads();
-  int wv=threadIdx.x>>6, ln=threadIdx.x&63;
-  int s=s0+wv;
-  const float* q=&fpsq[((size_t)b*SS+s)*3];
-  float qx=q[0],qy=q[1],qz=q[2];
-  float qn=__fadd_rn(__fadd_rn(__fmul_rn(qx,qx),__fmul_rn(qy,qy)),__fmul_rn(qz,qz));
-  f32x2 qxx,qyy,qzz,qnn,mtwo;
-  qxx.x=qx;qxx.y=qx; qyy.x=qy;qyy.y=qy; qzz.x=qz;qzz.y=qz; qnn.x=qn;qnn.y=qn;
-  mtwo.x=-2.f; mtwo.y=-2.f;
-  const float4* Xp=(const float4*)(xs+ln*KSTR);
-  const float4* Yp=(const float4*)(ys+ln*KSTR);
-  const float4* Zp=(const float4*)(zs+ln*KSTR);
-  const float4* Pp=(const float4*)(pn+ln*KSTR);
-  int base=ln*64;
-  u64 v[64];
-  #pragma unroll
-  for (int g=0;g<16;g++){
-    float4 x4=Xp[g], y4=Yp[g], z4=Zp[g], p4=Pp[g];
-    #pragma unroll
-    for (int h=0;h<2;h++){
-      f32x2 px2,py2,pz2,pn2;
-      if (h==0){ px2.x=x4.x;px2.y=x4.y; py2.x=y4.x;py2.y=y4.y; pz2.x=z4.x;pz2.y=z4.y; pn2.x=p4.x;pn2.y=p4.y; }
-      else     { px2.x=x4.z;px2.y=x4.w; py2.x=y4.z;py2.y=y4.w; pz2.x=z4.z;pz2.y=z4.w; pn2.x=p4.z;pn2.y=p4.w; }
-      f32x2 m1=pk_mul(qxx,px2);
-      f32x2 mm=pk_mul(qyy,py2);
-      f32x2 a1=pk_add(m1,mm);
-      f32x2 m3=pk_mul(qzz,pz2);
-      f32x2 dt=pk_add(a1,m3);
-      f32x2 qp=pk_add(qnn,pn2);
-      f32x2 nd=pk_mul(dt,mtwo);
-      f32x2 d2=pk_add(qp,nd);
-      #pragma unroll
-      for (int e=0;e<2;e++){
-        u32 bu=__float_as_uint(e?d2.y:d2.x);
-        bu = ((int)bu<0)? ~bu : (bu|0x80000000u);
-        v[g*4+h*2+e]=((u64)bu<<32)|(u32)(base+g*4+h*2+e);
-      }
-    }
-  }
-  u64 cand[8];
-  #pragma unroll
-  for (int gg=0;gg<8;gg++){
-    u64 c=v[gg*8];
-    #pragma unroll
-    for (int j=1;j<8;j++){ u64 x=v[gg*8+j]; c = x<c?x:c; }
-    cand[gg]=c;
-  }
-  u64 best=cand[0];
-  #pragma unroll
-  for (int gg=1;gg<8;gg++){ u64 x=cand[gg]; best = x<best?x:best; }
-  int my=0;
-  #pragma unroll 1
-  for (int r=0;r<KK;r++){
-    u64 w=best;
-    #pragma unroll
-    for (int m=1;m<64;m<<=1){ u64 o=__shfl_xor(w,m,64); w = o<w?o:w; }
-    if (ln==r) my=(int)(w&0xFFFull);
-    if (best==w){
-      #pragma unroll
-      for (int gg=0;gg<8;gg++){
-        if (cand[gg]==w){
-          u64 c=~0ull;
-          #pragma unroll
-          for (int j=0;j<8;j++){ u64 x=v[gg*8+j]; x = x>w ? x : ~0ull; c = x<c?x:c; }
-          cand[gg]=c;
-        }
-      }
-      u64 nb=cand[0];
-      #pragma unroll
-      for (int gg=1;gg<8;gg++){ u64 x=cand[gg]; nb = x<nb?x:nb; }
-      best=nb;
-    }
-  }
-  if (ln<KK) kidx[(((size_t)b*SS+s)<<5)+ln]=my;
-}
-
-__global__ __launch_bounds__(256) void k_l0(const float* __restrict__ xyz, const float* __restrict__ ft,
-    const float* __restrict__ fpsq, const int* __restrict__ kidx,
-    const float* __restrict__ w0t, const float* __restrict__ wt0,
-    u16* __restrict__ y0, float* __restrict__ wl0, float* __restrict__ statsf){
-  __shared__ u16 ytile[256][64];
-  __shared__ float pS[4][64], pQ[4][64];
-  __shared__ float pWS[4][8], pWQ[4][8];
-  int t=threadIdx.x; int wv=t>>6, ln=t&63;
-  int p=blockIdx.x*256+t;
-  int b=p>>15;
-  int site=p>>5;
-  int j=kidx[p];
-  const float* xb=xyz+(size_t)b*3*NN;
-  const float* q=fpsq+(size_t)site*3;
-  float gx=xb[j]-q[0], gy=xb[NN+j]-q[1], gz=xb[2*NN+j]-q[2];
-  float acc[64];
-  #pragma unroll
-  for (int c=0;c<64;c++) acc[c]=fmaf(gx,w0t[c],fmaf(gy,w0t[64+c],gz*w0t[128+c]));
-  const float4* fr=(const float4*)(ft+((size_t)b*NN+j)*64);
-  #pragma unroll 1
-  for (int kb=0;kb<4;kb++){
-    float4 r0=fr[kb*4+0], r1=fr[kb*4+1], r2=fr[kb*4+2], r3=fr[kb*4+3];
-    float ch[16]={r0.x,r0.y,r0.z,r0.w,r1.x,r1.y,r1.z,r1.w,r2.x,r2.y,r2.z,r2.w,r3.x,r3.y,r3.z,r3.w};
-    const float* wb=w0t+(3+kb*16)*64;
-    #pragma unroll
-    for (int kk=0;kk<16;kk++){
-      #pragma unroll
-      for (int c=0;c<64;c++) acc[c]=fmaf(ch[kk],wb[kk*64+c],acc[c]);
-    }
-  }
-  u16* yr=y0+(size_t)p*64;
-  #pragma unroll
-  for (int c8=0;c8<8;c8++){
-    uint4 pk=pack8(&acc[c8*8]);
-    ((uint4*)yr)[c8]=pk;
-    *((uint4*)&ytile[t][c8*8])=pk;
-  }
-  float wa[8];
-  #pragma unroll
-  for (int o=0;o<8;o++) wa[o]=fmaf(gx,wt0[o],fmaf(gy,wt0[8+o],gz*wt0[16+o]));
-  float4* wr=(float4*)(wl0+(size_t)p*8);
-  wr[0]=make_float4(wa[0],wa[1],wa[2],wa[3]);
-  wr[1]=make_float4(wa[4],wa[5],wa[6],wa[7]);
-  float wS[8],wQ[8];
-  #pragma unroll
-  for (int o=0;o<8;o++){
-    wS[o]=rl63(dppsum(wa[o]));
-    wQ[o]=rl63(dppsum(wa[o]*wa[o]));
-  }
-  if (ln==0){
-    #pragma unroll
-    for (int o=0;o<8;o++){ pWS[wv][o]=wS[o]; pWQ[wv][o]=wQ[o]; }
-  }
-  __syncthreads();
-  {
-    int c=t&63, rg=t>>6;
-    float S=0.f,Q=0.f;
-    #pragma unroll 16
-    for (int r=0;r<64;r++){
-      float v=bf2f((u32)ytile[rg*64+r][c]);
-      S+=v; Q=fmaf(v,v,Q);
-    }
-    pS[rg][c]=S; pQ[rg][c]=Q;
-  }
-  __syncthreads();
-  if (t<64){
-    float S=pS[0][t]+pS[1][t]+pS[2][t]+pS[3][t];
-    float Q=pQ[0][t]+pQ[1][t]+pQ[2][t]+pQ[3][t];
-    atomicAdd(&statsf[2*(ST_Y0+t)],S); atomicAdd(&statsf[2*(ST_Y0+t)+1],Q);
-  } else if (t<72){
-    int c=t-64;
-    float S=pWS[0][c]+pWS[1][c]+pWS[2][c]+pWS[3][c];
-    float Q=pWQ[0][c]+pWQ[1][c]+pWQ[2][c]+pWQ[3][c];
-    atomicAdd(&statsf[2*(ST_W0+c)],S); atomicAdd(&statsf[2*(ST_W0+c)+1],Q);
-  }
-}
-
-__global__ __launch_bounds__(256) void k_l1(const u16* __restrict__ y0, const float* __restrict__ wl0,
-    const float* __restrict__ w1t, const float* __restrict__ wt1,
-    const float* __restrict__ statsf,
-    const float* __restrict__ g0v, const float* __restrict__ be0v,
-    const float* __restrict__ wg0v, const float* __restrict__ wbe0v,
-    u16* __restrict__ y1, float* __restrict__ wl1, float* __restrict__ statso){
-  __shared__ float A0[64],C0[64],AW[8],CW[8];
-  __shared__ u16 ytile[256][64];
-  __shared__ float pS[4][64], pQ[4][64];
-  __shared__ float pWS[4][8], pWQ[4][8];
-  int t=threadIdx.x; int wv=t>>6, ln=t&63;
-  if (t<64){
-    float sm=statsf[(ST_Y0+t)*2], sq=statsf[(ST_Y0+t)*2+1];
-    float mean=sm*(1.f/PP), var=fmaxf(sq*(1.f/PP)-mean*mean,0.f);
-    float a=g0v[t]*rsqrtf(var+1e-5f); A0[t]=a; C0[t]=be0v[t]-mean*a;
-  } else if (t<72){
-    int c=t-64;
-    float sm=statsf[(ST_W0+c)*2], sq=statsf[(ST_W0+c)*2+1];
-    float mean=sm*(1.f/PP), var=fmaxf(sq*(1.f/PP)-mean*mean,0.f);
-    float a=wg0v[c]*rsqrtf(var+1e-5f); AW[c]=a; CW[c]=wbe0v[c]-mean*a;
-  }
-  __syncthreads();
-  int p=blockIdx.x*256+t;
-  const uint4* yr=(const uint4*)(y0+(size_t)p*64);
-  float acc[64];
-  #pragma unroll
-  for (int c=0;c<64;c++) acc[c]=0.f;
-  #pragma unroll 1
-  for (int kb=0;kb<4;kb++){
-    uint4 r0=yr[kb*2], r1=yr[kb*2+1];
-    float ch[16];
-    unp8_aff(r0,A0,C0,kb*16,ch);
-    unp8_aff(r1,A0,C0,kb*16+8,ch+8);
-    const float* wb=w1t+kb*16*64;
-    #pragma unroll
-    for (int kk=0;kk<16;kk++){
-      #pragma unroll
-      for (int c=0;c<64;c++) acc[c]=fmaf(ch[kk],wb[kk*64+c],acc[c]);
-    }
-  }
-  u16* yo=y1+(size_t)p*64;
-  #pragma unroll
-  for (int c8=0;c8<8;c8++){
-    uint4 pk=pack8(&acc[c8*8]);
-    ((uint4*)yo)[c8]=pk;
-    *((uint4*)&ytile[t][c8*8])=pk;
-  }
-  const float4* wvp=(const float4*)(wl0+(size_t)p*8);
-  float4 v0=wvp[0], v1=wvp[1];
-  float wi[8]={v0.x,v0.y,v0.z,v0.w,v1.x,v1.y,v1.z,v1.w};
-  float wo[8];
-  #pragma unroll
-  for (int o=0;o<8;o++) wo[o]=0.f;
-  #pragma unroll
-  for (int k=0;k<8;k++){
-    float xr=fmaxf(fmaf(wi[k],AW[k],CW[k]),0.f);
-    #pragma unroll
-    for (int o=0;o<8;o++) wo[o]=fmaf(xr,wt1[k*8+o],wo[o]);
-  }
-  float4* wr=(float4*)(wl1+(size_t)p*8);
-  wr[0]=make_float4(wo[0],wo[1],wo[2],wo[3]);
-  wr[1]=make_float4(wo[4],wo[5],wo[6],wo[7]);
-  float wS[8],wQ[8];
-  #pragma unroll
-  for (int o=0;o<8;o++){
-    wS[o]=rl63(dppsum(wo[o]));
-    wQ[o]=rl63(dppsum(wo[o]*wo[o]));
-  }
-  if (ln==0){
-    #pragma unroll
-    for (int o=0;o<8;o++){ pWS[wv][o]=wS[o]; pWQ[wv][o]=wQ[o]; }
-  }
-  __syncthreads();
-  {
-    int c=t&63, rg=t>>6;
-    float S=0.f,Q=0.f;
-    #pragma unroll 16
-    for (int r=0;r<64;r++){
-      float v=bf2f((u32)ytile[rg*64+r][c]);
-      S+=v; Q=fmaf(v,v,Q);
-    }
-    pS[rg][c]=S; pQ[rg][c]=Q;
-  }
-  __syncthreads();
-  if (t<64){
-    float S=pS[0][t]+pS[1][t]+pS[2][t]+pS[3][t];
-    float Q=pQ[0][t]+pQ[1][t]+pQ[2][t]+pQ[3][t];
-    atomicAdd(&statso[2*(ST_Y1+t)],S); atomicAdd(&statso[2*(ST_Y1+t)+1],Q);
-  } else if (t<72){
-    int c=t-64;
-    float S=pWS[0][c]+pWS[1][c]+pWS[2][c]+pWS[3][c];
-    float Q=pWQ[0][c]+pWQ[1][c]+pWQ[2][c]+pWQ[3][c];
-    atomicAdd(&statso[2*(ST_W1+c)],S); atomicAdd(&statso[2*(ST_W1+c)+1],Q);
-  }
-}
-
-__global__ __launch_bounds__(256) void k_l2(const u16* __restrict__ y1, const float* __restrict__ wl1,
-    const float* __restrict__ w2t, const float* __restrict__ wt2,
-    const float* __restrict__ statsf,
-    const float* __restrict__ g1v, const float* __restrict__ be1v,
-    const float* __restrict__ wg1v, const float* __restrict__ wbe1v,
-    u16* __restrict__ y2, float* __restrict__ wl2, float* __restrict__ statso){
-  __shared__ float A1[64],C1[64],AW[8],CW[8];
-  __shared__ u16 ytile[256][64];
-  __shared__ float pS[4][64], pQ[4][64];
-  __shared__ float pWS[4][16], pWQ[4][16];
-  int t=threadIdx.x; int wv=t>>6, ln=t&63;
-  if (t<64){
-    float sm=statsf[(ST_Y1+t)*2], sq=statsf[(ST_Y1+t)*2+1];
-    float mean=sm*(1.f/PP), var=fmaxf(sq*(1.f/PP)-mean*mean,0.f);
-    float a=g1v[t]*rsqrtf(var+1e-5f); A1[t]=a; C1[t]=be1v[t]-mean*a;
-  } else if (t<72){
-    int c=t-64;
-    float sm=statsf[(ST_W1+c)*2], sq=statsf[(ST_W1+c)*2+1];
-    float mean=sm*(1.f/PP), var=fmaxf(sq*(1.f/PP)-mean*mean,0.f);
-    float a=wg1v[c]*rsqrtf(var+1e-5f); AW[c]=a; CW[c]=wbe1v[c]-mean*a;
-  }
-  __syncthreads();
-  int p=blockIdx.x*256+t;
-  const uint4* yr=(const uint4*)(y1+(size_t)p*64);
-  #pragma unroll 1
-  for (int h=0;h<2;h++){
-    float acc[64];
-    #pragma unroll
-    for (int c=0;c<64;c++) acc[c]=0.f;
-    #pragma unroll 1
-    for (int kb=0;kb<4;kb++){
-      uint4 r0=yr[kb*2], r1=yr[kb*2+1];
-      float ch[16];
-      unp8_aff(r0,A1,C1,kb*16,ch);
-      unp8_aff(r1,A1,C1,kb*16+8,ch+8);
-      const float* wb=w2t+(size_t)kb*16*128+h*64;
-      #pragma unroll
-      for (int kk=0;kk<16;kk++){
-        #pragma unroll
-        for (int c=0;c<64;c++) acc[c]=fmaf(ch[kk],wb[kk*128+c],acc[c]);
-      }
-    }
-    u16* yo=y2+(size_t)p*128+h*64;
-    #pragma unroll
-    for (int c8=0;c8<8;c8++){
-      uint4 pk=pack8(&acc[c8*8]);
-      ((uint4*)yo)[c8]=pk;
-      *((uint4*)&ytile[t][c8*8])=pk;
-    }
-    __syncthreads();
-    {
-      int c=t&63, rg=t>>6;
-      float S=0.f,Q=0.f;
-      #pragma unroll 16
-      for (int r=0;r<64;r++){
-        float v=bf2f((u32)ytile[rg*64+r][c]);
-        S+=v; Q=fmaf(v,v,Q);
-      }
-      pS[rg][c]=S; pQ[rg][c]=Q;
-    }
-    __syncthreads();
-    if (t<64){
-      float S=pS[0][t]+pS[1][t]+pS[2][t]+pS[3][t];
-      float Q=pQ[0][t]+pQ[1][t]+pQ[2][t]+pQ[3][t];
-      atomicAdd(&statso[2*(ST_Y2+h*64+t)],S); atomicAdd(&statso[2*(ST_Y2+h*64+t)+1],Q);
-    }
-    __syncthreads();
-  }
-  const float4* wvp=(const float4*)(wl1+(size_t)p*8);
-  float4 v0=wvp[0], v1=wvp[1];
-  float wi[8]={v0.x,v0.y,v0.z,v0.w,v1.x,v1.y,v1.z,v1.w};
-  float wo[16];
-  #pragma unroll
-  for (int o=0;o<16;o++) wo[o]=0.f;
-  #pragma unroll
-  for (int k=0;k<8;k++){
-    float xr=fmaxf(fmaf(wi[k],AW[k],CW[k]),0.f);
-    #pragma unroll
-    for (int o=0;o<16;o++) wo[o]=fmaf(xr,wt2[k*16+o],wo[o]);
-  }
-  float4* wr=(float4*)(wl2+(size_t)p*16);
-  wr[0]=make_float4(wo[0],wo[1],wo[2],wo[3]);
-  wr[1]=make_float4(wo[4],wo[5],wo[6],wo[7]);
-  wr[2]=make_float4(wo[8],wo[9],wo[10],wo[11]);
-  wr[3]=make_float4(wo[12],wo[13],wo[14],wo[15]);
-  float wS[16],wQ[16];
-  #pragma unroll
-  for (int o=0;o<16;o++){
-    wS[o]=rl63(dppsum(wo[o]));
-    wQ[o]=rl63(dppsum(wo[o]*wo[o]));
-  }
-  if (ln==0){
-    #pragma unroll
-    for (int o=0;o<16;o++){ pWS[wv][o]=wS[o]; pWQ[wv][o]=wQ[o]; }
-  }
-  __syncthreads();
-  if (t<16){
-    float S=pWS[0][t]+pWS[1][t]+pWS[2][t]+pWS[3][t];
-    float Q=pWQ[0][t]+pWQ[1][t]+pWQ[2][t]+pWQ[3][t];
-    atomicAdd(&statso[2*(ST_W2+t)],S); atomicAdd(&statso[2*(ST_W2+t)+1],Q);
-  }
-}
-
-__global__ __launch_bounds__(256) void k_agg(const u16* __restrict__ y2, const float* __restrict__ wl2,
-    const float* __restrict__ statsf,
-    const float* __restrict__ g2v, const float* __restrict__ be2v,
-    const float* __restrict__ wg2v, const float* __restrict__ wbe2v,
-    u16* __restrict__ agg){
-  __shared__ float A2[128],C2[128],AW[16],CW[16];
-  __shared__ float nf[32*128];
-  __shared__ float wt[32*16];
-  int site=blockIdx.x; int t=threadIdx.x;
-  if (t<128){
-    float sm=statsf[(ST_Y2+t)*2], sq=statsf[(ST_Y2+t)*2+1];
-    float mean=sm*(1.f/PP), var=fmaxf(sq*(1.f/PP)-mean*mean,0.f);
-    float a=g2v[t]*rsqrtf(var+1e-5f); A2[t]=a; C2[t]=be2v[t]-mean*a;
-  } else if (t<144){
-    int c=t-128;
-    float sm=statsf[(ST_W2+c)*2], sq=statsf[(ST_W2+c)*2+1];
-    float mean=sm*(1.f/PP), var=fmaxf(sq*(1.f/PP)-mean*mean,0.f);
-    float a=wg2v[c]*rsqrtf(var+1e-5f); AW[c]=a; CW[c]=wbe2v[c]-mean*a;
-  }
-  __syncthreads();
-  const uint4* src=(const uint4*)(y2+(size_t)site*32*128);
-  #pragma unroll
-  for (int it=0;it<2;it++){
-    int idx=t+it*256;
-    uint4 r=src[idx];
-    int base=(idx*8)&127; int kq=(idx*8)>>7;
-    unp8_aff(r,A2,C2,base,&nf[kq*128+base]);
-  }
-  #pragma unroll
-  for (int it=0;it<2;it++){
-    int i=t+it*256;
-    float x=wl2[(size_t)site*512+i]; int c=i&15;
-    wt[i]=fmaxf(fmaf(x,AW[c],CW[c]),0.f);
-  }
-  __syncthreads();
-  int d=t>>1, cb=(t&1)*8;
-  float acc[8];
-  #pragma unroll
-  for (int e=0;e<8;e++) acc[e]=0.f;
-  #pragma unroll 4
-  for (int kq=0;kq<32;kq++){
-    float nv=nf[kq*128+d];
-    #pragma unroll
-    for (int e=0;e<8;e++) acc[e]=fmaf(nv,wt[kq*16+cb+e],acc[e]);
-  }
-  ((uint4*)(agg+(size_t)site*2048))[t]=pack8(acc);
-}
-
-__global__ __launch_bounds__(256) void k_lin(const u16* __restrict__ agg, const float* __restrict__ lw,
-                                             float* __restrict__ lin, float* __restrict__ outst){
-  __shared__ float As[32][33];
-  __shared__ float Bs[32][128];
-  __shared__ float stS[8][132], stQ[8][132];
-  int s0=blockIdx.x*32; int t=threadIdx.x;
-  int tx=t&31, ty=t>>5;
-  float acc[4][4];
-  #pragma unroll
-  for (int i=0;i<4;i++){
-    #pragma unroll
-    for (int jj=0;jj<4;jj++) acc[i][jj]=0.f;
-  }
-  for (int kb=0;kb<2048;kb+=32){
-    {
-      int row=t>>3, kc=(t&7)*4;
-      uint2 raw=*(const uint2*)(agg+((size_t)(s0+row))*2048+kb+kc);
-      As[row][kc  ]=bf2f(raw.x&0xffffu); As[row][kc+1]=bf2f(raw.x>>16);
-      As[row][kc+2]=bf2f(raw.y&0xffffu); As[row][kc+3]=bf2f(raw.y>>16);
-    }
-    {
-      int o=t>>1, ks=(t&1)*16;
-      const float* lr=lw+(size_t)o*2048+kb+ks;
-      #pragma unroll
-      for (int i=0;i<16;i+=4){
-        float4 r=*(const float4*)(lr+i);
-        Bs[ks+i][o]=r.x; Bs[ks+i+1][o]=r.y; Bs[ks+i+2][o]=r.z; Bs[ks+i+3][o]=r.w;
-      }
-    }
-    __syncthreads();
-    #pragma unroll 8
-    for (int kk=0;kk<32;kk++){
-      float av[4];
-      #pragma unroll
-      for (int i=0;i<4;i++) av[i]=As[ty*4+i][kk];
-      float4 bv=*(const float4*)(&Bs[kk][tx*4]);
-      #pragma unroll
-      for (int i=0;i<4;i++){
-        acc[i][0]=fmaf(av[i],bv.x,acc[i][0]);
-        acc[i][1]=fmaf(av[i],bv.y,acc[i][1]);
-        acc[i][2]=fmaf(av[i],bv.z,acc[i][2]);
-        acc[i][3]=fmaf(av[i],bv.w,acc[i][3]);
-      }
-    }
-    __syncthreads();
-  }
-  #pragma unroll
-  for (int i=0;i<4;i++){
-    float4 o4=make_float4(acc[i][0],acc[i][1],acc[i][2],acc[i][3]);
-    *(float4*)(lin+((size_t)(s0+ty*4+i))*128+tx*4)=o4;
-  }
-  #pragma unroll
-  for (int jj=0;jj<4;jj++){
-    float a0=acc[0][jj],a1=acc[1][jj],a2=acc[2][jj],a3=acc[3][jj];
-    stS[ty][tx*4+jj]=(a0+a1)+(a2+a3);
-    stQ[ty][tx*4+jj]=fmaf(a3,a3,fmaf(a2,a2,fmaf(a1,a1,a0*a0)));
-  }
-  __syncthreads();
-  if (t<128){
-    float S=0.f,Q=0.f;
-    #pragma unroll
-    for (int k=0;k<8;k++){ S+=stS[k][t]; Q+=stQ[k][t]; }
-    atomicAdd(&outst[2*t],S); atomicAdd(&outst[2*t+1],Q);
-  }
-}
-
-__global__ __launch_bounds__(256) void k_out(const float* __restrict__ lin, const float* __restrict__ statsf,
-    const float* __restrict__ lg, const float* __restrict__ lbe, float* __restrict__ outf){
-  int t=blockIdx.x*256+threadIdx.x;
-  int s4=(t&255)*4; int o=(t>>8)&127; int b=t>>15;
-  float sm=statsf[(ST_LIN+o)*2], sq=statsf[(ST_LIN+o)*2+1];
-  float mean=sm*(1.f/8192.f), var=fmaxf(sq*(1.f/8192.f)-mean*mean,0.f);
-  float a=lg[o]*rsqrtf(var+1e-5f), cc=lbe[o]-mean*a;
-  float v0=lin[((size_t)b*SS+s4+0)*128+o];
-  float v1=lin[((size_t)b*SS+s4+1)*128+o];
-  float v2=lin[((size_t)b*SS+s4+2)*128+o];
-  float v3=lin[((size_t)b*SS+s4+3)*128+o];
-  float4 r=make_float4(fmaxf(fmaf(v0,a,cc),0.f),fmaxf(fmaf(v1,a,cc),0.f),
-                       fmaxf(fmaf(v2,a,cc),0.f),fmaxf(fmaf(v3,a,cc),0.f));
-  *(float4*)(outf+((size_t)b*128+o)*SS+s4)=r;
 }
 
 extern "C" void kernel_launch(void* const* d_in, const int* in_sizes, int n_in,
@@ -731,17 +748,23 @@
   float* ft=(float*)(ws+o_ft);
   u16* y0=(u16*)(ws+o_y0); u16* y1=(u16*)(ws+o_y1); u16* y2=(u16*)(ws+o_y2);
   float* wl0=(float*)(ws+o_wl0); float* wl1=(float*)(ws+o_wl1); float* wl2=(float*)(ws+o_wl2);
-  u16* agg=(u16*)(ws+o_agg); float* lin=(float*)(ws+o_lin);
-
-  size_t knn_smem = (size_t)4*64*KSTR*4;
-
-  hipLaunchKernelGGL(k_fps_ft,dim3(265),dim3(512),0,stream,xyz,fpsq,out,feat,ft,
-                     w0,w1,w2,ww0,ww1,ww2,w0t,w1t,w2t,wt0,wt1,wt2,statsf);
-  hipLaunchKernelGGL(k_knn,dim3(2048),dim3(256),knn_smem,stream,xyz,fpsq,kidx);
-  hipLaunchKernelGGL(k_l0,dim3(PP/256),dim3(256),0,stream,xyz,ft,fpsq,kidx,w0t,wt0,y0,wl0,statsf);
-  hipLaunchKernelGGL(k_l1,dim3(PP/256),dim3(256),0,stream,y0,wl0,w1t,wt1,statsf,g0,be0,wg0,wbe0,y1,wl1,statsf);
-  hipLaunchKernelGGL(k_l2,dim3(PP/256),dim3(256),0,stream,y1,wl1,w2t,wt2,statsf,g1,be1,wg1,wbe1,y2,wl2,statsf);
-  hipLaunchKernelGGL(k_agg,dim3(8192),dim3(256),0,stream,y2,wl2,statsf,g2,be2,wg2,wbe2,agg);
-  hipLaunchKernelGGL(k_lin,dim3(256),dim3(256),0,stream,agg,lw,lin,statsf+2*ST_LIN);
-  hipLaunchKernelGGL(k_out,dim3(1024),dim3(256),0,stream,lin,statsf,lg,lbe,out+BB*3*SS);
-}
+  u16* aggb=(u16*)(ws+o_agg); float* lin=(float*)(ws+o_lin);
+
+  void* kargs[]={
+    (void*)&xyz,(void*)&feat,
+    (void*)&w0,(void*)&w1,(void*)&w2,
+    (void*)&ww0,(void*)&ww1,(void*)&ww2,
+    (void*)&g0,(void*)&be0,(void*)&g1,(void*)&be1,(void*)&g2,(void*)&be2,
+    (void*)&wg0,(void*)&wbe0,(void*)&wg1,(void*)&wbe1,(void*)&wg2,(void*)&wbe2,
+    (void*)&lw,(void*)&lg,(void*)&lbe,
+    (void*)&out,
+    (void*)&fpsq,(void*)&kidx,(void*)&ft,
+    (void*)&y0,(void*)&y1,(void*)&y2,
+    (void*)&wl0,(void*)&wl1,(void*)&wl2,
+    (void*)&aggb,(void*)&lin,(void*)&statsf,
+    (void*)&w0t,(void*)&w1t,(void*)&w2t,
+    (void*)&wt0,(void*)&wt1,(void*)&wt2
+  };
+  (void)hipLaunchCooperativeKernel((const void*)k_mega, dim3(256), dim3(512),
+                                   kargs, DLDS, stream);
+}
```
